# Kernel optimization log

Measured on AMD Instinct MI355X. Metric: run time of the kernel, lower is better.

The kernel has to match this reference:

```python
import jax, jax.numpy as jnp
import numpy as np

NB, H = 4, 16
EPS = 1e-5


def _ln(x, w=None, b=None):
    m = jnp.mean(x, -1, keepdims=True)
    v = jnp.var(x, -1, keepdims=True)
    y = (x - m) * jax.lax.rsqrt(v + EPS)
    if w is not None:
        y = y * w
    if b is not None:
        y = y + b
    return y


def _ada_ln(a, s, ln_s_w, w_gamma, w_beta):
    # AF3 Algorithm 26: a <- sigmoid(Lin(LN_nobias(s))) * LN_noaffine(a) + Lin(LN_nobias(s))
    a_n = _ln(a)
    s_n = _ln(s, ln_s_w)
    return jax.nn.sigmoid(s_n @ w_gamma) * a_n + s_n @ w_beta


def setup_inputs():
    key = jax.random.key(0)
    B, S, c_a, c_s, c_z = 1, 1024, 768, 384, 128
    n_hidden = 2 * c_a  # expansion factor n=2
    ks = iter(jax.random.split(key, 40))

    def rn(shape, scale=1.0):
        return scale * jax.random.normal(next(ks), shape, dtype=jnp.float32)

    p = 0.02
    return {
        "a": rn((B, S, c_a)),
        "s": rn((B, S, c_s)),
        "z": rn((B, S, S, c_z)),
        "beta": rn((B, S, S, H)),
        # per-block AttentionPairBias params (stacked over NB blocks)
        "ln_s_w_attn": jnp.ones((NB, c_s)),
        "wg_attn": rn((NB, c_s, c_a), p),
        "wb_attn": rn((NB, c_s, c_a), p),
        "wq": rn((NB, c_a, c_a), p),
        "bq": jnp.zeros((NB, c_a)),
        "wk": rn((NB, c_a, c_a), p),
        "wv": rn((NB, c_a, c_a), p),
        "ln_z_w": jnp.ones((NB, c_z)),
        "ln_z_b": jnp.zeros((NB, c_z)),
        "wpb": rn((NB, c_z, H), p),
        "wgate": rn((NB, c_a, c_a), p),
        "wo": rn((NB, c_a, c_a), p),
        "wsg_attn": rn((NB, c_s, c_a), p),
        "bsg_attn": -2.0 * jnp.ones((NB, c_a)),
        # per-block ConditionedTransitionBlock params
        "ln_s_w_tr": jnp.ones((NB, c_s)),
        "wg_tr": rn((NB, c_s, c_a), p),
        "wb_tr": rn((NB, c_s, c_a), p),
        "w_swish": rn((NB, c_a, n_hidden), p),
        "w_gate2": rn((NB, c_a, n_hidden), p),
        "wsg_tr": rn((NB, c_s, c_a), p),
        "bsg_tr": -2.0 * jnp.ones((NB, c_a)),
        "w_out": rn((NB, n_hidden, c_a), p),
    }


def reference(a, s, z, beta, ln_s_w_attn, wg_attn, wb_attn, wq, bq, wk, wv,
              ln_z_w, ln_z_b, wpb, wgate, wo, wsg_attn, bsg_attn,
              ln_s_w_tr, wg_tr, wb_tr, w_swish, w_gate2, wsg_tr, bsg_tr, w_out):
    B, S, c_a = a.shape
    d = c_a // H
    scale = 1.0 / jnp.sqrt(jnp.float32(d))
    for i in range(NB):
        # --- AttentionPairBias (AF3 Alg 24) ---
        ah = _ada_ln(a, s, ln_s_w_attn[i], wg_attn[i], wb_attn[i])
        q = (ah @ wq[i] + bq[i]).reshape(B, S, H, d)
        k = (ah @ wk[i]).reshape(B, S, H, d)
        v = (ah @ wv[i]).reshape(B, S, H, d)
        zb = _ln(z, ln_z_w[i], ln_z_b[i]) @ wpb[i]  # [B,S,S,H] pair bias
        scores = jnp.einsum('bihd,bjhd->bhij', q, k) * scale \
                 + jnp.transpose(zb + beta, (0, 3, 1, 2))
        attn = jax.nn.softmax(scores, axis=-1)
        o = jnp.einsum('bhij,bjhd->bihd', attn, v)
        g = jax.nn.sigmoid(ah @ wgate[i]).reshape(B, S, H, d)
        att_out = (g * o).reshape(B, S, c_a) @ wo[i]
        b_attn = jax.nn.sigmoid(s @ wsg_attn[i] + bsg_attn[i]) * att_out
        # --- ConditionedTransitionBlock (AF3 Alg 25, SwiGLU) ---
        th = _ada_ln(a, s, ln_s_w_tr[i], wg_tr[i], wb_tr[i])
        hidden = jax.nn.silu(th @ w_swish[i]) * (th @ w_gate2[i])
        tr = jax.nn.sigmoid(s @ wsg_tr[i] + bsg_tr[i]) * (hidden @ w_out[i])
        a = b_attn + tr
    return a
```

## Files before the change

### kernel.cpp

```cpp
#include <hip/hip_runtime.h>
#include <hip/hip_bf16.h>

typedef __hip_bfloat16 bf16;
typedef __attribute__((ext_vector_type(8))) short s8v;
typedef __attribute__((ext_vector_type(4))) float f4v;

constexpr int S = 1024, CA = 768, CS = 384, CZ = 128, NHID = 1536;
constexpr int NBLK = 4, NHEAD = 16, DH = 48;
constexpr float EPS = 1e-5f;

#define DEV static __device__ __forceinline__

DEV float sigmoidf_(float x) { return 1.0f / (1.0f + __expf(-x)); }

DEV f4v mfma16(s8v a, s8v b, f4v c) {
  return __builtin_amdgcn_mfma_f32_16x16x32_bf16(a, b, c, 0, 0, 0);
}

DEV void gld_lds16(const void* g, void* l) {
  __builtin_amdgcn_global_load_lds((const __attribute__((address_space(1))) void*)g,
                                   (__attribute__((address_space(3))) void*)l, 16, 0, 0);
}

union U8 { s8v s; bf16 h[8]; };
union U4 { uint2 u; bf16 h[4]; };

DEV float wred_sum(float v) {
#pragma unroll
  for (int o = 32; o; o >>= 1) v += __shfl_xor(v, o);
  return v;
}

__global__ __launch_bounds__(256) void rowln_s(const float* __restrict__ x,
                                               bf16* __restrict__ s_hat,
                                               bf16* __restrict__ s_bf) {
  constexpr int C = CS, C4 = C / 4;
  __shared__ float red[8];
  const int t = threadIdx.x;
  const size_t row = blockIdx.x;
  float4 v = make_float4(0.f, 0.f, 0.f, 0.f);
  if (t < C4) v = ((const float4*)(x + row * C))[t];
  float sum = v.x + v.y + v.z + v.w;
  float sq = v.x * v.x + v.y * v.y + v.z * v.z + v.w * v.w;
  sum = wred_sum(sum); sq = wred_sum(sq);
  const int wv = t >> 6;
  if ((t & 63) == 0) { red[2 * wv] = sum; red[2 * wv + 1] = sq; }
  __syncthreads();
  sum = red[0] + red[2] + red[4] + red[6];
  sq = red[1] + red[3] + red[5] + red[7];
  const float m = sum / C;
  const float rstd = rsqrtf(sq / C - m * m + EPS);
  if (t < C4) {
    U4 oh, ob_;
    oh.h[0] = __float2bfloat16((v.x - m) * rstd); oh.h[1] = __float2bfloat16((v.y - m) * rstd);
    oh.h[2] = __float2bfloat16((v.z - m) * rstd); oh.h[3] = __float2bfloat16((v.w - m) * rstd);
    ob_.h[0] = __float2bfloat16(v.x); ob_.h[1] = __float2bfloat16(v.y);
    ob_.h[2] = __float2bfloat16(v.z); ob_.h[3] = __float2bfloat16(v.w);
    *(uint2*)(s_hat + row * C + 4 * t) = oh.u;
    *(uint2*)(s_bf + row * C + 4 * t) = ob_.u;
  }
}

__global__ __launch_bounds__(256) void ln_adaln2(const float* __restrict__ a,
                                                 const bf16* __restrict__ ada,
                                                 bf16* __restrict__ ah_attn,
                                                 bf16* __restrict__ ah_tr) {
  __shared__ float red[8];
  const int t = threadIdx.x;
  const size_t row = blockIdx.x;
  float4 v = make_float4(0.f, 0.f, 0.f, 0.f);
  if (t < 192) v = ((const float4*)(a + row * CA))[t];
  float sum = v.x + v.y + v.z + v.w;
  float sq = v.x * v.x + v.y * v.y + v.z * v.z + v.w * v.w;
  sum = wred_sum(sum); sq = wred_sum(sq);
  const int wv = t >> 6;
  if ((t & 63) == 0) { red[2 * wv] = sum; red[2 * wv + 1] = sq; }
  __syncthreads();
  sum = red[0] + red[2] + red[4] + red[6];
  sq = red[1] + red[3] + red[5] + red[7];
  const float m = sum / CA;
  const float rstd = rsqrtf(sq / CA - m * m + EPS);
  if (t < 192) {
    const float an[4] = {(v.x - m) * rstd, (v.y - m) * rstd, (v.z - m) * rstd, (v.w - m) * rstd};
    const bf16* ar = ada + row * 12288 + 4 * t;
    U4 g1, b1, g2, b2, o1, o2;
    g1.u = *(const uint2*)(ar);
    b1.u = *(const uint2*)(ar + 768);
    g2.u = *(const uint2*)(ar + 1536);
    b2.u = *(const uint2*)(ar + 2304);
#pragma unroll
    for (int j = 0; j < 4; ++j) {
      o1.h[j] = __float2bfloat16(sigmoidf_(__bfloat162float(g1.h[j])) * an[j] + __bfloat162float(b1.h[j]));
      o2.h[j] = __float2bfloat16(sigmoidf_(__bfloat162float(g2.h[j])) * an[j] + __bfloat162float(b2.h[j]));
    }
    *(uint2*)(ah_attn + row * CA + 4 * t) = o1.u;
    *(uint2*)(ah_tr + row * CA + 4 * t) = o2.u;
  }
}

__global__ __launch_bounds__(256) void final_adaln(const float* __restrict__ sg,
                                                   const bf16* __restrict__ att,
                                                   const bf16* __restrict__ tr,
                                                   const bf16* __restrict__ ada,
                                                   bf16* __restrict__ ah_attn,
                                                   bf16* __restrict__ ah_tr) {
  __shared__ float red[8];
  const int t = threadIdx.x;
  const size_t row = blockIdx.x;
  float o[4] = {0.f, 0.f, 0.f, 0.f};
  if (t < 192) {
    const float4 sa = *(const float4*)(sg + row * 6144 + 4 * t);
    const float4 st = *(const float4*)(sg + row * 6144 + 768 + 4 * t);
    U4 av, tv;
    av.u = *(const uint2*)(att + row * CA + 4 * t);
    tv.u = *(const uint2*)(tr + row * CA + 4 * t);
    o[0] = sa.x * __bfloat162float(av.h[0]) + st.x * __bfloat162float(tv.h[0]);
    o[1] = sa.y * __bfloat162float(av.h[1]) + st.y * __bfloat162float(tv.h[1]);
    o[2] = sa.z * __bfloat162float(av.h[2]) + st.z * __bfloat162float(tv.h[2]);
    o[3] = sa.w * __bfloat162float(av.h[3]) + st.w * __bfloat162float(tv.h[3]);
  }
  float sum = o[0] + o[1] + o[2] + o[3];
  float sq = o[0] * o[0] + o[1] * o[1] + o[2] * o[2] + o[3] * o[3];
  sum = wred_sum(sum); sq = wred_sum(sq);
  const int wv = t >> 6;
  if ((t & 63) == 0) { red[2 * wv] = sum; red[2 * wv + 1] = sq; }
  __syncthreads();
  sum = red[0] + red[2] + red[4] + red[6];
  sq = red[1] + red[3] + red[5] + red[7];
  const float m = sum / CA;
  const float rstd = rsqrtf(sq / CA - m * m + EPS);
  if (t < 192) {
    const bf16* ar = ada + row * 12288 + 4 * t;
    U4 g1, b1, g2, b2, o1, o2;
    g1.u = *(const uint2*)(ar);
    b1.u = *(const uint2*)(ar + 768);
    g2.u = *(const uint2*)(ar + 1536);
    b2.u = *(const uint2*)(ar + 2304);
#pragma unroll
    for (int j = 0; j < 4; ++j) {
      const float an = (o[j] - m) * rstd;
      o1.h[j] = __float2bfloat16(sigmoidf_(__bfloat162float(g1.h[j])) * an + __bfloat162float(b1.h[j]));
      o2.h[j] = __float2bfloat16(sigmoidf_(__bfloat162float(g2.h[j])) * an + __bfloat162float(b2.h[j]));
    }
    *(uint2*)(ah_attn + row * CA + 4 * t) = o1.u;
    *(uint2*)(ah_tr + row * CA + 4 * t) = o2.u;
  }
}

struct TGroup {
  const float* src[6];
  bf16* dst[6];
  const float* cs[6];
  long dstZ[6];
};

__global__ __launch_bounds__(256) void transpose_grp(TGroup g, int K, int N, int csZ) {
  __shared__ float tile[32][33];
  const int z = blockIdx.z, wsel = z >> 2, blk = z & 3;
  const float* src = g.src[wsel] + (size_t)blk * K * N;
  bf16* dst = g.dst[wsel] + (size_t)blk * g.dstZ[wsel];
  const float* cs = g.cs[wsel];
  const int k0 = blockIdx.y * 32, n0 = blockIdx.x * 32;
  const int tx = threadIdx.x & 31, ty = threadIdx.x >> 5;
#pragma unroll
  for (int q = 0; q < 4; ++q) {
    const int k = k0 + ty + 8 * q;
    float v = src[(size_t)k * N + n0 + tx];
    if (cs) v *= cs[(size_t)blk * csZ + k];
    tile[ty + 8 * q][tx] = v;
  }
  __syncthreads();
#pragma unroll
  for (int q = 0; q < 4; ++q)
    dst[(size_t)(n0 + ty + 8 * q) * K + k0 + tx] = __float2bfloat16(tile[tx][ty + 8 * q]);
}

__global__ __launch_bounds__(256) void prep_all(const float* __restrict__ ln_z_w,
                                                const float* __restrict__ ln_z_b,
                                                const float* __restrict__ wpb,
                                                bf16* __restrict__ W2T,
                                                float* __restrict__ bias2,
                                                const float* __restrict__ bq,
                                                const float* __restrict__ bsg_attn,
                                                const float* __restrict__ bsg_tr,
                                                float* __restrict__ biasQKVG,
                                                float* __restrict__ biasSG) {
  const int blk = blockIdx.x;
  const int t = threadIdx.x;
  if (blk == 48) {
    for (int f = t; f < 64 * CZ; f += 256) {
      const int col = f >> 7, c = f & 127, b = col >> 4, h = col & 15;
      W2T[f] = __float2bfloat16(ln_z_w[b * CZ + c] * wpb[(b * CZ + c) * NHEAD + h]);
    }
    if (t < 64) {
      const int b = t >> 4, h = t & 15;
      float sum = 0.f;
      for (int c = 0; c < CZ; ++c)
        sum += ln_z_b[b * CZ + c] * wpb[(b * CZ + c) * NHEAD + h];
      bias2[t] = sum;
    }
    return;
  }
  const int g = blk * 256 + t;
  if (g < 4 * 3072) {
    const int b = g / 3072, c = g % 3072;
    biasQKVG[g] = (c < 768) ? bq[b * 768 + c] : 0.f;
  }
  if (g < 6144) {
    const int b = g / 1536, c = g % 1536;
    biasSG[g] = (c < 768) ? bsg_attn[b * 768 + c] : bsg_tr[b * 768 + c - 768];
  }
}

__global__ __launch_bounds__(256) void zbias_kernel(const float* __restrict__ z,
                                                    const float* __restrict__ beta,
                                                    const bf16* __restrict__ W2T,
                                                    const float* __restrict__ bias2,
                                                    bf16* __restrict__ bias_all) {
  __shared__ s8v zt8[64 * 16];
  __shared__ s8v w2s[64 * 16];
  __shared__ float betas[64][17];
  __shared__ float bias2s[64];
  __shared__ bf16 obuf[64][72];
  const int t = threadIdx.x;
  const int i = blockIdx.y, j0 = blockIdx.x * 64;
#pragma unroll
  for (int q = 0; q < 4; ++q) {
    const int u = q * 256 + t;
    const int row = u >> 4, sl = u & 15;
    w2s[row * 16 + (sl ^ (row & 7))] = *(const s8v*)(W2T + row * CZ + sl * 8);
  }
  if (t < 64) bias2s[t] = bias2[t];
  {
    const int j = t >> 2, h4 = t & 3;
    const float4 bv = *(const float4*)(beta + ((size_t)i * S + j0 + j) * NHEAD + 4 * h4);
    betas[j][4 * h4 + 0] = bv.x; betas[j][4 * h4 + 1] = bv.y;
    betas[j][4 * h4 + 2] = bv.z; betas[j][4 * h4 + 3] = bv.w;
  }
  {
    const int p = t >> 2, q = t & 3;
    const float* zr = z + ((size_t)i * S + j0 + p) * CZ + q * 32;
    float vals[32];
    float sum = 0.f, sq = 0.f;
#pragma unroll
    for (int k4 = 0; k4 < 8; ++k4) {
      const float4 xv = *(const float4*)(zr + 4 * k4);
      vals[4 * k4 + 0] = xv.x; vals[4 * k4 + 1] = xv.y;
      vals[4 * k4 + 2] = xv.z; vals[4 * k4 + 3] = xv.w;
      sum += xv.x + xv.y + xv.z + xv.w;
      sq += xv.x * xv.x + xv.y * xv.y + xv.z * xv.z + xv.w * xv.w;
    }
    sum += __shfl_xor(sum, 1); sum += __shfl_xor(sum, 2);
    sq += __shfl_xor(sq, 1); sq += __shfl_xor(sq, 2);
    const float m = sum / CZ;
    const float rstd = rsqrtf(sq / CZ - m * m + EPS);
#pragma unroll
    for (int u = 0; u < 4; ++u) {
      U8 pk;
#pragma unroll
      for (int e = 0; e < 8; ++e) pk.h[e] = __float2bfloat16((vals[8 * u + e] - m) * rstd);
      const int cu = 4 * q + u;
      zt8[p * 16 + (cu ^ (p & 7))] = pk.s;
    }
  }
  __syncthreads();
  const int lane = t & 63, wid = t >> 6;
  const int wr = wid >> 1, wc = wid & 1;
  const int ln = lane & 15, lq = lane >> 4;
  f4v acc[2][2] = {};
#pragma unroll
  for (int kk = 0; kk < 4; ++kk) {
    const int sl = (lq + 4 * kk) ^ (ln & 7);
    s8v a[2], b[2];
#pragma unroll
    for (int mi = 0; mi < 2; ++mi) a[mi] = zt8[(32 * wr + 16 * mi + ln) * 16 + sl];
#pragma unroll
    for (int ni = 0; ni < 2; ++ni) b[ni] = w2s[(32 * wc + 16 * ni + ln) * 16 + sl];
#pragma unroll
    for (int mi = 0; mi < 2; ++mi)
#pragma unroll
      for (int ni = 0; ni < 2; ++ni) acc[mi][ni] = mfma16(a[mi], b[ni], acc[mi][ni]);
  }
#pragma unroll
  for (int mi = 0; mi < 2; ++mi)
#pragma unroll
    for (int ni = 0; ni < 2; ++ni) {
      const int col = 32 * wc + 16 * ni + ln;
      const int jb = 32 * wr + 16 * mi + 4 * lq;
      U4 o4;
#pragma unroll
      for (int r = 0; r < 4; ++r)
        o4.h[r] = __float2bfloat16(acc[mi][ni][r] + bias2s[col] + betas[jb + r][col & 15]);
      *(uint2*)&obuf[col][jb] = o4.u;
    }
  __syncthreads();
  {
    const int oc = t >> 2, js = (t & 3) * 16;
    bf16* dp = bias_all + (size_t)oc * S * S + (size_t)i * S + j0 + js;
    *(s8v*)dp = *(const s8v*)&obuf[oc][js];
    *(s8v*)(dp + 8) = *(const s8v*)&obuf[oc][js + 8];
  }
}

struct Gemm2Args {
  const bf16* A0[2]; int lda0[2];
  const bf16* Bt[2];
  const float* bias[2];
  void* C[2];
  int K[2];
  int nb[2];
  int outMode[2];
  int N[2];
  bf16* vT;
};

__global__ __launch_bounds__(256) void gemm2(Gemm2Args ga) {
  const int z = blockIdx.z;
  if ((int)blockIdx.x >= ga.nb[z]) return;
  __shared__ s8v As[1024];
  __shared__ s8v Bs[1024];
  const bf16* A0 = ga.A0[z]; const int lda0 = ga.lda0[z];
  const bf16* Bt = ga.Bt[z];
  const int K = ga.K[z], N = ga.N[z];
  const int t = threadIdx.x;
  const int lane = t & 63, wid = t >> 6;
  const int wr = wid >> 1, wc = wid & 1;
  const int ln = lane & 15, lq = lane >> 4;
  const int m0 = blockIdx.y * 128, n0 = blockIdx.x * 128;
  int rowA[4], colx[4];
#pragma unroll
  for (int q = 0; q < 4; ++q) {
    const int u = q * 256 + t, row = u >> 3, slp = u & 7;
    rowA[q] = row; colx[q] = (slp ^ (row & 7)) * 8;
  }
  f4v acc[4][4] = {};
  for (int ks = 0; ks < K; ks += 64) {
    __syncthreads();
#pragma unroll
    for (int q = 0; q < 4; ++q) {
      gld_lds16(A0 + (size_t)(m0 + rowA[q]) * lda0 + ks + colx[q], &As[q * 256 + wid * 64]);
      gld_lds16(Bt + (size_t)(n0 + rowA[q]) * K + ks + colx[q], &Bs[q * 256 + wid * 64]);
    }
    __syncthreads();
#pragma unroll
    for (int kk = 0; kk < 2; ++kk) {
      const int sl = (lq + 4 * kk) ^ (ln & 7);
      s8v a[4], b[4];
#pragma unroll
      for (int mi = 0; mi < 4; ++mi) a[mi] = As[(64 * wr + 16 * mi + ln) * 8 + sl];
#pragma unroll
      for (int ni = 0; ni < 4; ++ni) b[ni] = Bs[(64 * wc + 16 * ni + ln) * 8 + sl];
#pragma unroll
      for (int mi = 0; mi < 4; ++mi)
#pragma unroll
        for (int ni = 0; ni < 4; ++ni) acc[mi][ni] = mfma16(a[mi], b[ni], acc[mi][ni]);
    }
  }
  const bool vdiv = (ga.vT != nullptr) && (z == 0) && (n0 >= 1536) && (n0 < 2304);
  const int om = ga.outMode[z];
#pragma unroll
  for (int ni = 0; ni < 4; ++ni) {
    const int n = n0 + 64 * wc + 16 * ni + ln;
    const float bv = ga.bias[z] ? ga.bias[z][n] : 0.f;
#pragma unroll
    for (int mi = 0; mi < 4; ++mi) {
      const int mb = m0 + 64 * wr + 16 * mi + 4 * lq;
      if (vdiv) {
        U4 o4;
#pragma unroll
        for (int r = 0; r < 4; ++r) o4.h[r] = __float2bfloat16(acc[mi][ni][r] + bv);
        *(uint2*)(ga.vT + (size_t)(n - 1536) * S + mb) = o4.u;
      } else if (om == 0) {
        bf16* C = (bf16*)ga.C[z];
#pragma unroll
        for (int r = 0; r < 4; ++r)
          C[(size_t)(mb + r) * N + n] = __float2bfloat16(acc[mi][ni][r] + bv);
      } else {
        float* C = (float*)ga.C[z];
#pragma unroll
        for (int r = 0; r < 4; ++r)
          C[(size_t)(mb + r) * N + n] = sigmoidf_(acc[mi][ni][r] + bv);
      }
    }
  }
}

struct GemmPairArgs {
  const bf16* A0[2]; int lda0[2];
  const bf16* A1[2]; int lda1[2];
  const bf16* Bt[2];
  const float* bias[2];
  bf16* C[2];
  int K[2]; int amode[2];
};

DEV s8v combineRT(s8v x, s8v y, int amode) {
  U8 ux, uy, r;
  ux.s = x; uy.s = y;
#pragma unroll
  for (int j = 0; j < 8; ++j) {
    const float fx = __bfloat162float(ux.h[j]);
    const float fy = __bfloat162float(uy.h[j]);
    const float tt = sigmoidf_(fx);
    r.h[j] = __float2bfloat16((amode == 2 ? fx * tt : tt) * fy);
  }
  return r.s;
}

__global__ __launch_bounds__(256) void gemm_pair(GemmPairArgs ga, int N) {
  __shared__ s8v As[128 * 8];
  __shared__ s8v Bs[128 * 8];
  const int z = blockIdx.z;
  const bf16* A0 = ga.A0[z]; const int lda0 = ga.lda0[z];
  const bf16* A1 = ga.A1[z]; const int lda1 = ga.lda1[z];
  const bf16* Bt = ga.Bt[z];
  const float* bias = ga.bias[z];
  bf16* C = ga.C[z];
  const int K = ga.K[z], amode = ga.amode[z];
  const int t = threadIdx.x;
  const int lane = t & 63, wid = t >> 6;
  const int wr = wid >> 1, wc = wid & 1;
  const int ln = lane & 15, lq = lane >> 4;
  const int m0 = blockIdx.y * 128, n0 = blockIdx.x * 128;
  int rowS[4], slS[4], swz[4];
#pragma unroll
  for (int q = 0; q < 4; ++q) {
    const int u = q * 256 + t;
    rowS[q] = u >> 3; slS[q] = u & 7;
    swz[q] = rowS[q] * 8 + (slS[q] ^ (rowS[q] & 7));
  }
  f4v acc[4][4] = {};
  s8v ra[4], ra2[4], rb[4];
#pragma unroll
  for (int q = 0; q < 4; ++q) {
    ra[q] = *(const s8v*)(A0 + (size_t)(m0 + rowS[q]) * lda0 + slS[q] * 8);
    if (amode != 0) ra2[q] = *(const s8v*)(A1 + (size_t)(m0 + rowS[q]) * lda1 + slS[q] * 8);
    rb[q] = *(const s8v*)(Bt + (size_t)(n0 + rowS[q]) * K + slS[q] * 8);
  }
  for (int ks = 0;;) {
    __syncthreads();
#pragma unroll
    for (int q = 0; q < 4; ++q) {
      As[swz[q]] = (amode == 0) ? ra[q] : combineRT(ra[q], ra2[q], amode);
      Bs[swz[q]] = rb[q];
    }
    const int ksn = ks + 64;
    if (ksn < K) {
#pragma unroll
      for (int q = 0; q < 4; ++q) {
        ra[q] = *(const s8v*)(A0 + (size_t)(m0 + rowS[q]) * lda0 + ksn + slS[q] * 8);
        if (amode != 0) ra2[q] = *(const s8v*)(A1 + (size_t)(m0 + rowS[q]) * lda1 + ksn + slS[q] * 8);
        rb[q] = *(const s8v*)(Bt + (size_t)(n0 + rowS[q]) * K + ksn + slS[q] * 8);
      }
    }
    __syncthreads();
#pragma unroll
    for (int kk = 0; kk < 2; ++kk) {
      const int sl = (lq + 4 * kk) ^ (ln & 7);
      s8v a[4], b[4];
#pragma unroll
      for (int mi = 0; mi < 4; ++mi) a[mi] = As[(64 * wr + 16 * mi + ln) * 8 + sl];
#pragma unroll
      for (int ni = 0; ni < 4; ++ni) b[ni] = Bs[(64 * wc + 16 * ni + ln) * 8 + sl];
#pragma unroll
      for (int mi = 0; mi < 4; ++mi)
#pragma unroll
        for (int ni = 0; ni < 4; ++ni) acc[mi][ni] = mfma16(a[mi], b[ni], acc[mi][ni]);
    }
    ks = ksn;
    if (ks >= K) break;
  }
#pragma unroll
  for (int ni = 0; ni < 4; ++ni) {
    const int n = n0 + 64 * wc + 16 * ni + ln;
    const float bv = bias ? bias[n] : 0.f;
#pragma unroll
    for (int mi = 0; mi < 4; ++mi) {
      const int mb = m0 + 64 * wr + 16 * mi + 4 * lq;
#pragma unroll
      for (int r = 0; r < 4; ++r)
        C[(size_t)(mb + r) * N + n] = __float2bfloat16(acc[mi][ni][r] + bv);
    }
  }
}

__global__ __launch_bounds__(256) void flash_attn(const bf16* __restrict__ qkvg,
                                                  const bf16* __restrict__ vT,
                                                  const bf16* __restrict__ bias_all,
                                                  bf16* __restrict__ ob, int blk) {
  __shared__ s8v Qs[64 * 8];
  __shared__ s8v Ks[2][64 * 8];
  __shared__ s8v Vs[2][48 * 8];
  __shared__ s8v Bs[2][64 * 8];
  __shared__ bf16 PwB[4 * 1024];
  __shared__ float facL[4][16];
  __shared__ float linvL[4][16];
  const int t = threadIdx.x;
  const int lane = t & 63, w = t >> 6;
  const int ln = lane & 15, lq = lane >> 4;
  const int h = blockIdx.y, i0 = blockIdx.x * 64;
  const bf16* bp = bias_all + (size_t)(blk * NHEAD + h) * S * S;
  const float scale = 0.14433756729740643f;

#pragma unroll
  for (int uu = 0; uu < 2; ++uu) {
    const int u = t + 256 * uu, row = u >> 3, sl = u & 7;
    s8v qv{};
    if (sl < 6) qv = *(const s8v*)(qkvg + (size_t)(i0 + row) * 3072 + h * DH + sl * 8);
    Qs[row * 8 + (sl ^ (row & 7))] = qv;
  }

  s8v kr[2], br[2], vr0{}, vr1{};
  auto prefetch = [&](int jt) {
    const int j0 = jt * 64;
#pragma unroll
    for (int uu = 0; uu < 2; ++uu) {
      const int u = t + 256 * uu, row = u >> 3, sl = u & 7;
      s8v kv{};
      if (sl < 6) kv = *(const s8v*)(qkvg + (size_t)(j0 + row) * 3072 + 768 + h * DH + sl * 8);
      kr[uu] = kv;
      br[uu] = *(const s8v*)(bp + (size_t)(i0 + row) * S + j0 + sl * 8);
    }
    { const int d = t >> 3, sl = t & 7;
      vr0 = *(const s8v*)(vT + (size_t)(h * DH + d) * S + j0 + sl * 8); }
    if (t < 128) {
      const int u = 256 + t, d = u >> 3, sl = u & 7;
      vr1 = *(const s8v*)(vT + (size_t)(h * DH + d) * S + j0 + sl * 8);
    }
  };
  auto store_tiles = [&](int pb) {
#pragma unroll
    for (int uu = 0; uu < 2; ++uu) {
      const int u = t + 256 * uu, row = u >> 3, sl = u & 7;
      const int ph = row * 8 + (sl ^ (row & 7));
      Ks[pb][ph] = kr[uu];
      Bs[pb][ph] = br[uu];
    }
    { const int d = t >> 3, sl = t & 7;
      Vs[pb][d * 8 + (sl ^ (d & 7))] = vr0; }
    if (t < 128) {
      const int u = 256 + t, d = u >> 3, sl = u & 7;
      Vs[pb][d * 8 + (sl ^ (d & 7))] = vr1;
    }
  };

  float m_run = -3e30f, l_run = 0.f;
  f4v acc_o[3] = {};
  bf16* pw = PwB + w * 1024;

  prefetch(0);
  for (int jt = 0; jt < 16; ++jt) {
    const int pb = jt & 1;
    __syncthreads();
    store_tiles(pb);
    __syncthreads();
    if (jt < 15) prefetch(jt + 1);
    float p[4][4];
    float tmax = -3e30f;
#pragma unroll
    for (int ja = 0; ja < 4; ++ja) {
      f4v accs = {};
#pragma unroll
      for (int ks2 = 0; ks2 < 2; ++ks2) {
        const int sl = (lq + 4 * ks2) ^ (ln & 7);
        const s8v a = Ks[pb][(16 * ja + ln) * 8 + sl];
        const s8v b = Qs[(16 * w + ln) * 8 + sl];
        accs = mfma16(a, b, accs);
      }
      const int jq = 4 * ja + lq;
      const int pu = jq >> 1;
      U4 bv;
      bv.u = *(const uint2*)((const bf16*)(&Bs[pb][0]) +
                             (((16 * w + ln) * 8 + (pu ^ (ln & 7))) * 8 + (jq & 1) * 4));
#pragma unroll
      for (int r = 0; r < 4; ++r) {
        p[ja][r] = accs[r] * scale + __bfloat162float(bv.h[r]);
        tmax = fmaxf(tmax, p[ja][r]);
      }
    }
    tmax = fmaxf(tmax, __shfl_xor(tmax, 16));
    tmax = fmaxf(tmax, __shfl_xor(tmax, 32));
    const float m_new = fmaxf(m_run, tmax);
    const float fac = __expf(m_run - m_new);
    m_run = m_new;
    float psum = 0.f;
#pragma unroll
    for (int ja = 0; ja < 4; ++ja)
#pragma unroll
      for (int r = 0; r < 4; ++r) {
        p[ja][r] = __expf(p[ja][r] - m_new);
        psum += p[ja][r];
      }
    psum += __shfl_xor(psum, 16);
    psum += __shfl_xor(psum, 32);
    l_run = l_run * fac + psum;
    if (lq == 0) facL[w][ln] = fac;
#pragma unroll
    for (int ja = 0; ja < 4; ++ja) {
      const int ju = 4 * ja + lq;
      const int ph = ju ^ ((ln & 7) << 1);
      U4 pk;
#pragma unroll
      for (int r = 0; r < 4; ++r) pk.h[r] = __float2bfloat16(p[ja][r]);
      *(uint2*)(pw + ln * 64 + ph * 4) = pk.u;
    }
    asm volatile("s_waitcnt lgkmcnt(0)" ::: "memory");
    __builtin_amdgcn_sched_barrier(0);
    const float4 fv = *(const float4*)&facL[w][4 * lq];
#pragma unroll
    for (int ni = 0; ni < 3; ++ni) {
      acc_o[ni][0] *= fv.x; acc_o[ni][1] *= fv.y;
      acc_o[ni][2] *= fv.z; acc_o[ni][3] *= fv.w;
    }
#pragma unroll
    for (int ks2 = 0; ks2 < 2; ++ks2) {
      const int pu0 = (2 * lq + 8 * ks2) ^ ((ln & 7) << 1);
      const s8v pa = *(const s8v*)(pw + ln * 64 + pu0 * 4);
      const int slv = (lq + 4 * ks2) ^ (ln & 7);
#pragma unroll
      for (int ni = 0; ni < 3; ++ni) {
        const s8v vb = Vs[pb][(16 * ni + ln) * 8 + slv];
        acc_o[ni] = mfma16(pa, vb, acc_o[ni]);
      }
    }
  }
  if (lq == 0) linvL[w][ln] = 1.0f / l_run;
  asm volatile("s_waitcnt lgkmcnt(0)" ::: "memory");
  __builtin_amdgcn_sched_barrier(0);
  const float4 lv = *(const float4*)&linvL[w][4 * lq];
  const float lvr[4] = {lv.x, lv.y, lv.z, lv.w};
#pragma unroll
  for (int ni = 0; ni < 3; ++ni)
#pragma unroll
    for (int r = 0; r < 4; ++r) {
      const int m = i0 + 16 * w + 4 * lq + r;
      ob[(size_t)m * CA + h * DH + 16 * ni + ln] = __float2bfloat16(acc_o[ni][r] * lvr[r]);
    }
}

__global__ __launch_bounds__(256) void ew_final(const float* __restrict__ sg,
                                                const bf16* __restrict__ att,
                                                const bf16* __restrict__ tr,
                                                float* __restrict__ out) {
  const int i = blockIdx.x * 256 + threadIdx.x;
  const int row = i / 192, col = (i % 192) * 4;
  const float4 sa = *(const float4*)(sg + (size_t)row * 6144 + col);
  const float4 st = *(const float4*)(sg + (size_t)row * 6144 + 768 + col);
  U4 av, tv;
  av.u = *(const uint2*)(att + (size_t)row * CA + col);
  tv.u = *(const uint2*)(tr + (size_t)row * CA + col);
  float4 o;
  o.x = sa.x * __bfloat162float(av.h[0]) + st.x * __bfloat162float(tv.h[0]);
  o.y = sa.y * __bfloat162float(av.h[1]) + st.y * __bfloat162float(tv.h[1]);
  o.z = sa.z * __bfloat162float(av.h[2]) + st.z * __bfloat162float(tv.h[2]);
  o.w = sa.w * __bfloat162float(av.h[3]) + st.w * __bfloat162float(tv.h[3]);
  *(float4*)(out + (size_t)row * CA + col) = o;
}

__global__ void fill_kernel(float* p, int n, float v) {
  const int i = blockIdx.x * 256 + threadIdx.x;
  if (i < n) p[i] = v;
}

extern "C" void kernel_launch(void* const* d_in, const int* in_sizes, int n_in,
                              void* d_out, int out_size, void* d_ws, size_t ws_size,
                              hipStream_t stream) {
  (void)in_sizes; (void)n_in;
  const float* a_in = (const float*)d_in[0];
  const float* s_in = (const float*)d_in[1];
  const float* z_in = (const float*)d_in[2];
  const float* beta = (const float*)d_in[3];
  const float* ln_s_w_attn = (const float*)d_in[4];
  const float* wg_attn = (const float*)d_in[5];
  const float* wb_attn = (const float*)d_in[6];
  const float* wq = (const float*)d_in[7];
  const float* bq = (const float*)d_in[8];
  const float* wk = (const float*)d_in[9];
  const float* wv = (const float*)d_in[10];
  const float* ln_z_w = (const float*)d_in[11];
  const float* ln_z_b = (const float*)d_in[12];
  const float* wpb = (const float*)d_in[13];
  const float* wgate = (const float*)d_in[14];
  const float* wo = (const float*)d_in[15];
  const float* wsg_attn = (const float*)d_in[16];
  const float* bsg_attn = (const float*)d_in[17];
  const float* ln_s_w_tr = (const float*)d_in[18];
  const float* wg_tr = (const float*)d_in[19];
  const float* wb_tr = (const float*)d_in[20];
  const float* w_swish = (const float*)d_in[21];
  const float* w_gate2 = (const float*)d_in[22];
  const float* wsg_tr = (const float*)d_in[23];
  const float* bsg_tr = (const float*)d_in[24];
  const float* w_out = (const float*)d_in[25];

  char* wp = (char*)d_ws;
  size_t used = 0;
  auto alloc = [&](size_t bytes) -> void* {
    void* p = wp + used;
    used += (bytes + 255) & ~(size_t)255;
    return p;
  };
  bf16* bias_all = (bf16*)alloc((size_t)64 * S * S * 2);
  bf16* WT_ada = (bf16*)alloc((size_t)4 * 3072 * 384 * 2);
  bf16* WT_sg = (bf16*)alloc((size_t)4 * 1536 * 384 * 2);
  bf16* WT_qkvg = (bf16*)alloc((size_t)4 * 3072 * 768 * 2);
  bf16* WT_wo = (bf16*)alloc((size_t)4 * 768 * 768 * 2);
  bf16* WT_mlp = (bf16*)alloc((size_t)4 * 3072 * 768 * 2);
  bf16* WT_wout = (bf16*)alloc((size_t)4 * 768 * 1536 * 2);
  float* biasQKVG = (float*)alloc(4 * 3072 * 4);
  float* biasSG = (float*)alloc(6144 * 4);
  bf16* W2T = (bf16*)alloc(64 * 128 * 2);
  float* bias2 = (float*)alloc(64 * 4);
  bf16* ada_all = (bf16*)alloc((size_t)S * 12288 * 2);
  float* sg_all = (float*)alloc((size_t)S * 6144 * 4);
  bf16* s_hat = (bf16*)alloc((size_t)S * CS * 2);
  bf16* s_bf = (bf16*)alloc((size_t)S * CS * 2);
  bf16* ah_attn = (bf16*)alloc((size_t)S * CA * 2);
  bf16* ah_tr = (bf16*)alloc((size_t)S * CA * 2);
  bf16* qkvg = (bf16*)alloc((size_t)S * 3072 * 2);
  bf16* vT = (bf16*)alloc((size_t)CA * S * 2);
  bf16* ob = (bf16*)alloc((size_t)S * CA * 2);
  bf16* att = (bf16*)alloc((size_t)S * CA * 2);
  bf16* swg = (bf16*)alloc((size_t)S * 3072 * 2);
  bf16* trout = (bf16*)alloc((size_t)S * CA * 2);
  if (used > ws_size) {
    fill_kernel<<<(out_size + 255) / 256, 256, 0, stream>>>((float*)d_out, out_size, 12345.0f);
    return;
  }

  const dim3 B256(256);

  prep_all<<<49, B256, 0, stream>>>(ln_z_w, ln_z_b, wpb, W2T, bias2,
                                    bq, bsg_attn, bsg_tr, biasQKVG, biasSG);

  {
    TGroup g{};
    g.src[0] = wg_attn;  g.dst[0] = WT_ada + (size_t)0 * 384;    g.cs[0] = ln_s_w_attn; g.dstZ[0] = 3072 * 384;
    g.src[1] = wb_attn;  g.dst[1] = WT_ada + (size_t)768 * 384;  g.cs[1] = ln_s_w_attn; g.dstZ[1] = 3072 * 384;
    g.src[2] = wg_tr;    g.dst[2] = WT_ada + (size_t)1536 * 384; g.cs[2] = ln_s_w_tr;   g.dstZ[2] = 3072 * 384;
    g.src[3] = wb_tr;    g.dst[3] = WT_ada + (size_t)2304 * 384; g.cs[3] = ln_s_w_tr;   g.dstZ[3] = 3072 * 384;
    g.src[4] = wsg_attn; g.dst[4] = WT_sg + (size_t)0 * 384;     g.cs[4] = nullptr;     g.dstZ[4] = 1536 * 384;
    g.src[5] = wsg_tr;   g.dst[5] = WT_sg + (size_t)768 * 384;   g.cs[5] = nullptr;     g.dstZ[5] = 1536 * 384;
    transpose_grp<<<dim3(24, 12, 24), B256, 0, stream>>>(g, 384, 768, CS);
  }
  {
    TGroup g{};
    g.src[0] = wq;    g.dst[0] = WT_qkvg + (size_t)0 * 768;    g.dstZ[0] = 3072 * 768;
    g.src[1] = wk;    g.dst[1] = WT_qkvg + (size_t)768 * 768;  g.dstZ[1] = 3072 * 768;
    g.src[2] = wv;    g.dst[2] = WT_qkvg + (size_t)1536 * 768; g.dstZ[2] = 3072 * 768;
    g.src[3] = wgate; g.dst[3] = WT_qkvg + (size_t)2304 * 768; g.dstZ[3] = 3072 * 768;
    g.src[4] = wo;    g.dst[4] = WT_wo;                        g.dstZ[4] = 768 * 768;
    transpose_grp<<<dim3(24, 24, 20), B256, 0, stream>>>(g, 768, 768, 0);
  }
  {
    TGroup g{};
    g.src[0] = w_swish; g.dst[0] = WT_mlp + (size_t)0 * 768;    g.dstZ[0] = 3072 * 768;
    g.src[1] = w_gate2; g.dst[1] = WT_mlp + (size_t)1536 * 768; g.dstZ[1] = 3072 * 768;
    transpose_grp<<<dim3(48, 24, 8), B256, 0, stream>>>(g, 768, 1536, 0);
  }
  {
    TGroup g{};
    g.src[0] = w_out; g.dst[0] = WT_wout; g.dstZ[0] = 768 * 1536;
    transpose_grp<<<dim3(24, 48, 4), B256, 0, stream>>>(g, 1536, 768, 0);
  }

  rowln_s<<<S, B256, 0, stream>>>(s_in, s_hat, s_bf);
  zbias_kernel<<<dim3(16, 1024), B256, 0, stream>>>(z_in, beta, W2T, bias2, bias_all);

  {
    Gemm2Args ga{};
    ga.A0[0] = s_hat; ga.lda0[0] = 384; ga.Bt[0] = WT_ada; ga.bias[0] = nullptr;
    ga.C[0] = ada_all; ga.K[0] = 384; ga.nb[0] = 96; ga.outMode[0] = 0; ga.N[0] = 12288;
    ga.A0[1] = s_bf; ga.lda0[1] = 384; ga.Bt[1] = WT_sg; ga.bias[1] = biasSG;
    ga.C[1] = sg_all; ga.K[1] = 384; ga.nb[1] = 48; ga.outMode[1] = 1; ga.N[1] = 6144;
    ga.vT = nullptr;
    gemm2<<<dim3(96, 8, 2), B256, 0, stream>>>(ga);
  }

  ln_adaln2<<<S, B256, 0, stream>>>(a_in, ada_all, ah_attn, ah_tr);
  for (int b = 0; b < NBLK; ++b) {
    {
      Gemm2Args ga{};
      ga.A0[0] = ah_attn; ga.lda0[0] = 768; ga.Bt[0] = WT_qkvg + (size_t)b * 3072 * 768;
      ga.bias[0] = biasQKVG + b * 3072; ga.C[0] = qkvg; ga.K[0] = 768; ga.nb[0] = 24;
      ga.outMode[0] = 0; ga.N[0] = 3072;
      ga.A0[1] = ah_tr; ga.lda0[1] = 768; ga.Bt[1] = WT_mlp + (size_t)b * 3072 * 768;
      ga.bias[1] = nullptr; ga.C[1] = swg; ga.K[1] = 768; ga.nb[1] = 24;
      ga.outMode[1] = 0; ga.N[1] = 3072;
      ga.vT = vT;
      gemm2<<<dim3(24, 8, 2), B256, 0, stream>>>(ga);
    }
    flash_attn<<<dim3(16, 16), B256, 0, stream>>>(qkvg, vT, bias_all, ob, b);
    {
      GemmPairArgs ga{};
      ga.A0[0] = qkvg + 2304; ga.lda0[0] = 3072; ga.A1[0] = ob; ga.lda1[0] = 768;
      ga.Bt[0] = WT_wo + (size_t)b * 768 * 768; ga.bias[0] = nullptr;
      ga.C[0] = att; ga.K[0] = 768; ga.amode[0] = 1;
      ga.A0[1] = swg; ga.lda0[1] = 3072; ga.A1[1] = swg + 1536; ga.lda1[1] = 3072;
      ga.Bt[1] = WT_wout + (size_t)b * 768 * 1536; ga.bias[1] = nullptr;
      ga.C[1] = trout; ga.K[1] = 1536; ga.amode[1] = 2;
      gemm_pair<<<dim3(6, 8, 2), B256, 0, stream>>>(ga, 768);
    }
    if (b < NBLK - 1) {
      final_adaln<<<S, B256, 0, stream>>>(sg_all + (size_t)b * 1536, att, trout,
                                          ada_all + (size_t)(b + 1) * 3072, ah_attn, ah_tr);
    } else {
      ew_final<<<768, B256, 0, stream>>>(sg_all + (size_t)b * 1536, att, trout, (float*)d_out);
    }
  }
}
```

Measured before the change: 676.6 us.

## Split flash attention over key halves and unify GEMMs with smaller M tiles

Flash attention now runs as two key-range halves per query tile, writing partial fp32 outputs and (max, sum) stats that a new combine kernel merges into the normalized bf16 output. This doubles the number of attention workgroups from 256 to 512 to better fill the GPU. All GEMMs go through a single gemmA kernel whose grid uses 16 row blocks instead of 8, so each tile covers 64 rows and more blocks run at once. The cost is an extra kernel launch, fp32 partial output traffic, and possibly less data reuse per GEMM tile.

```diff
diff --git a/kernel.cpp b/kernel.cpp
--- a/kernel.cpp
+++ b/kernel.cpp
@@ -15,11 +15,6 @@
 
 DEV f4v mfma16(s8v a, s8v b, f4v c) {
   return __builtin_amdgcn_mfma_f32_16x16x32_bf16(a, b, c, 0, 0, 0);
-}
-
-DEV void gld_lds16(const void* g, void* l) {
-  __builtin_amdgcn_global_load_lds((const __attribute__((address_space(1))) void*)g,
-                                   (__attribute__((address_space(3))) void*)l, 16, 0, 0);
 }
 
 union U8 { s8v s; bf16 h[8]; };
@@ -147,497 +142,6 @@
   }
 }
 
-struct TGroup {
-  const float* src[6];
-  bf16* dst[6];
-  const float* cs[6];
-  long dstZ[6];
-};
-
-__global__ __launch_bounds__(256) void transpose_grp(TGroup g, int K, int N, int csZ) {
-  __shared__ float tile[32][33];
-  const int z = blockIdx.z, wsel = z >> 2, blk = z & 3;
-  const float* src = g.src[wsel] + (size_t)blk * K * N;
-  bf16* dst = g.dst[wsel] + (size_t)blk * g.dstZ[wsel];
-  const float* cs = g.cs[wsel];
-  const int k0 = blockIdx.y * 32, n0 = blockIdx.x * 32;
-  const int tx = threadIdx.x & 31, ty = threadIdx.x >> 5;
-#pragma unroll
-  for (int q = 0; q < 4; ++q) {
-    const int k = k0 + ty + 8 * q;
-    float v = src[(size_t)k * N + n0 + tx];
-    if (cs) v *= cs[(size_t)blk * csZ + k];
-    tile[ty + 8 * q][tx] = v;
-  }
-  __syncthreads();
-#pragma unroll
-  for (int q = 0; q < 4; ++q)
-    dst[(size_t)(n0 + ty + 8 * q) * K + k0 + tx] = __float2bfloat16(tile[tx][ty + 8 * q]);
-}
-
-__global__ __launch_bounds__(256) void prep_all(const float* __restrict__ ln_z_w,
-                                                const float* __restrict__ ln_z_b,
-                                                const float* __restrict__ wpb,
-                                                bf16* __restrict__ W2T,
-                                                float* __restrict__ bias2,
-                                                const float* __restrict__ bq,
-                                                const float* __restrict__ bsg_attn,
-                                                const float* __restrict__ bsg_tr,
-                                                float* __restrict__ biasQKVG,
-                                                float* __restrict__ biasSG) {
-  const int blk = blockIdx.x;
-  const int t = threadIdx.x;
-  if (blk == 48) {
-    for (int f = t; f < 64 * CZ; f += 256) {
-      const int col = f >> 7, c = f & 127, b = col >> 4, h = col & 15;
-      W2T[f] = __float2bfloat16(ln_z_w[b * CZ + c] * wpb[(b * CZ + c) * NHEAD + h]);
-    }
-    if (t < 64) {
-      const int b = t >> 4, h = t & 15;
-      float sum = 0.f;
-      for (int c = 0; c < CZ; ++c)
-        sum += ln_z_b[b * CZ + c] * wpb[(b * CZ + c) * NHEAD + h];
-      bias2[t] = sum;
-    }
-    return;
-  }
-  const int g = blk * 256 + t;
-  if (g < 4 * 3072) {
-    const int b = g / 3072, c = g % 3072;
-    biasQKVG[g] = (c < 768) ? bq[b * 768 + c] : 0.f;
-  }
-  if (g < 6144) {
-    const int b = g / 1536, c = g % 1536;
-    biasSG[g] = (c < 768) ? bsg_attn[b * 768 + c] : bsg_tr[b * 768 + c - 768];
-  }
-}
-
-__global__ __launch_bounds__(256) void zbias_kernel(const float* __restrict__ z,
-                                                    const float* __restrict__ beta,
-                                                    const bf16* __restrict__ W2T,
-                                                    const float* __restrict__ bias2,
-                                                    bf16* __restrict__ bias_all) {
-  __shared__ s8v zt8[64 * 16];
-  __shared__ s8v w2s[64 * 16];
-  __shared__ float betas[64][17];
-  __shared__ float bias2s[64];
-  __shared__ bf16 obuf[64][72];
-  const int t = threadIdx.x;
-  const int i = blockIdx.y, j0 = blockIdx.x * 64;
-#pragma unroll
-  for (int q = 0; q < 4; ++q) {
-    const int u = q * 256 + t;
-    const int row = u >> 4, sl = u & 15;
-    w2s[row * 16 + (sl ^ (row & 7))] = *(const s8v*)(W2T + row * CZ + sl * 8);
-  }
-  if (t < 64) bias2s[t] = bias2[t];
-  {
-    const int j = t >> 2, h4 = t & 3;
-    const float4 bv = *(const float4*)(beta + ((size_t)i * S + j0 + j) * NHEAD + 4 * h4);
-    betas[j][4 * h4 + 0] = bv.x; betas[j][4 * h4 + 1] = bv.y;
-    betas[j][4 * h4 + 2] = bv.z; betas[j][4 * h4 + 3] = bv.w;
-  }
-  {
-    const int p = t >> 2, q = t & 3;
-    const float* zr = z + ((size_t)i * S + j0 + p) * CZ + q * 32;
-    float vals[32];
-    float sum = 0.f, sq = 0.f;
-#pragma unroll
-    for (int k4 = 0; k4 < 8; ++k4) {
-      const float4 xv = *(const float4*)(zr + 4 * k4);
-      vals[4 * k4 + 0] = xv.x; vals[4 * k4 + 1] = xv.y;
-      vals[4 * k4 + 2] = xv.z; vals[4 * k4 + 3] = xv.w;
-      sum += xv.x + xv.y + xv.z + xv.w;
-      sq += xv.x * xv.x + xv.y * xv.y + xv.z * xv.z + xv.w * xv.w;
-    }
-    sum += __shfl_xor(sum, 1); sum += __shfl_xor(sum, 2);
-    sq += __shfl_xor(sq, 1); sq += __shfl_xor(sq, 2);
-    const float m = sum / CZ;
-    const float rstd = rsqrtf(sq / CZ - m * m + EPS);
-#pragma unroll
-    for (int u = 0; u < 4; ++u) {
-      U8 pk;
-#pragma unroll
-      for (int e = 0; e < 8; ++e) pk.h[e] = __float2bfloat16((vals[8 * u + e] - m) * rstd);
-      const int cu = 4 * q + u;
-      zt8[p * 16 + (cu ^ (p & 7))] = pk.s;
-    }
-  }
-  __syncthreads();
-  const int lane = t & 63, wid = t >> 6;
-  const int wr = wid >> 1, wc = wid & 1;
-  const int ln = lane & 15, lq = lane >> 4;
-  f4v acc[2][2] = {};
-#pragma unroll
-  for (int kk = 0; kk < 4; ++kk) {
-    const int sl = (lq + 4 * kk) ^ (ln & 7);
-    s8v a[2], b[2];
-#pragma unroll
-    for (int mi = 0; mi < 2; ++mi) a[mi] = zt8[(32 * wr + 16 * mi + ln) * 16 + sl];
-#pragma unroll
-    for (int ni = 0; ni < 2; ++ni) b[ni] = w2s[(32 * wc + 16 * ni + ln) * 16 + sl];
-#pragma unroll
-    for (int mi = 0; mi < 2; ++mi)
-#pragma unroll
-      for (int ni = 0; ni < 2; ++ni) acc[mi][ni] = mfma16(a[mi], b[ni], acc[mi][ni]);
-  }
-#pragma unroll
-  for (int mi = 0; mi < 2; ++mi)
-#pragma unroll
-    for (int ni = 0; ni < 2; ++ni) {
-      const int col = 32 * wc + 16 * ni + ln;
-      const int jb = 32 * wr + 16 * mi + 4 * lq;
-      U4 o4;
-#pragma unroll
-      for (int r = 0; r < 4; ++r)
-        o4.h[r] = __float2bfloat16(acc[mi][ni][r] + bias2s[col] + betas[jb + r][col & 15]);
-      *(uint2*)&obuf[col][jb] = o4.u;
-    }
-  __syncthreads();
-  {
-    const int oc = t >> 2, js = (t & 3) * 16;
-    bf16* dp = bias_all + (size_t)oc * S * S + (size_t)i * S + j0 + js;
-    *(s8v*)dp = *(const s8v*)&obuf[oc][js];
-    *(s8v*)(dp + 8) = *(const s8v*)&obuf[oc][js + 8];
-  }
-}
-
-struct Gemm2Args {
-  const bf16* A0[2]; int lda0[2];
-  const bf16* Bt[2];
-  const float* bias[2];
-  void* C[2];
-  int K[2];
-  int nb[2];
-  int outMode[2];
-  int N[2];
-  bf16* vT;
-};
-
-__global__ __launch_bounds__(256) void gemm2(Gemm2Args ga) {
-  const int z = blockIdx.z;
-  if ((int)blockIdx.x >= ga.nb[z]) return;
-  __shared__ s8v As[1024];
-  __shared__ s8v Bs[1024];
-  const bf16* A0 = ga.A0[z]; const int lda0 = ga.lda0[z];
-  const bf16* Bt = ga.Bt[z];
-  const int K = ga.K[z], N = ga.N[z];
-  const int t = threadIdx.x;
-  const int lane = t & 63, wid = t >> 6;
-  const int wr = wid >> 1, wc = wid & 1;
-  const int ln = lane & 15, lq = lane >> 4;
-  const int m0 = blockIdx.y * 128, n0 = blockIdx.x * 128;
-  int rowA[4], colx[4];
-#pragma unroll
-  for (int q = 0; q < 4; ++q) {
-    const int u = q * 256 + t, row = u >> 3, slp = u & 7;
-    rowA[q] = row; colx[q] = (slp ^ (row & 7)) * 8;
-  }
-  f4v acc[4][4] = {};
-  for (int ks = 0; ks < K; ks += 64) {
-    __syncthreads();
-#pragma unroll
-    for (int q = 0; q < 4; ++q) {
-      gld_lds16(A0 + (size_t)(m0 + rowA[q]) * lda0 + ks + colx[q], &As[q * 256 + wid * 64]);
-      gld_lds16(Bt + (size_t)(n0 + rowA[q]) * K + ks + colx[q], &Bs[q * 256 + wid * 64]);
-    }
-    __syncthreads();
-#pragma unroll
-    for (int kk = 0; kk < 2; ++kk) {
-      const int sl = (lq + 4 * kk) ^ (ln & 7);
-      s8v a[4], b[4];
-#pragma unroll
-      for (int mi = 0; mi < 4; ++mi) a[mi] = As[(64 * wr + 16 * mi + ln) * 8 + sl];
-#pragma unroll
-      for (int ni = 0; ni < 4; ++ni) b[ni] = Bs[(64 * wc + 16 * ni + ln) * 8 + sl];
-#pragma unroll
-      for (int mi = 0; mi < 4; ++mi)
-#pragma unroll
-        for (int ni = 0; ni < 4; ++ni) acc[mi][ni] = mfma16(a[mi], b[ni], acc[mi][ni]);
-    }
-  }
-  const bool vdiv = (ga.vT != nullptr) && (z == 0) && (n0 >= 1536) && (n0 < 2304);
-  const int om = ga.outMode[z];
-#pragma unroll
-  for (int ni = 0; ni < 4; ++ni) {
-    const int n = n0 + 64 * wc + 16 * ni + ln;
-    const float bv = ga.bias[z] ? ga.bias[z][n] : 0.f;
-#pragma unroll
-    for (int mi = 0; mi < 4; ++mi) {
-      const int mb = m0 + 64 * wr + 16 * mi + 4 * lq;
-      if (vdiv) {
-        U4 o4;
-#pragma unroll
-        for (int r = 0; r < 4; ++r) o4.h[r] = __float2bfloat16(acc[mi][ni][r] + bv);
-        *(uint2*)(ga.vT + (size_t)(n - 1536) * S + mb) = o4.u;
-      } else if (om == 0) {
-        bf16* C = (bf16*)ga.C[z];
-#pragma unroll
-        for (int r = 0; r < 4; ++r)
-          C[(size_t)(mb + r) * N + n] = __float2bfloat16(acc[mi][ni][r] + bv);
-      } else {
-        float* C = (float*)ga.C[z];
-#pragma unroll
-        for (int r = 0; r < 4; ++r)
-          C[(size_t)(mb + r) * N + n] = sigmoidf_(acc[mi][ni][r] + bv);
-      }
-    }
-  }
-}
-
-struct GemmPairArgs {
-  const bf16* A0[2]; int lda0[2];
-  const bf16* A1[2]; int lda1[2];
-  const bf16* Bt[2];
-  const float* bias[2];
-  bf16* C[2];
-  int K[2]; int amode[2];
-};
-
-DEV s8v combineRT(s8v x, s8v y, int amode) {
-  U8 ux, uy, r;
-  ux.s = x; uy.s = y;
-#pragma unroll
-  for (int j = 0; j < 8; ++j) {
-    const float fx = __bfloat162float(ux.h[j]);
-    const float fy = __bfloat162float(uy.h[j]);
-    const float tt = sigmoidf_(fx);
-    r.h[j] = __float2bfloat16((amode == 2 ? fx * tt : tt) * fy);
-  }
-  return r.s;
-}
-
-__global__ __launch_bounds__(256) void gemm_pair(GemmPairArgs ga, int N) {
-  __shared__ s8v As[128 * 8];
-  __shared__ s8v Bs[128 * 8];
-  const int z = blockIdx.z;
-  const bf16* A0 = ga.A0[z]; const int lda0 = ga.lda0[z];
-  const bf16* A1 = ga.A1[z]; const int lda1 = ga.lda1[z];
-  const bf16* Bt = ga.Bt[z];
-  const float* bias = ga.bias[z];
-  bf16* C = ga.C[z];
-  const int K = ga.K[z], amode = ga.amode[z];
-  const int t = threadIdx.x;
-  const int lane = t & 63, wid = t >> 6;
-  const int wr = wid >> 1, wc = wid & 1;
-  const int ln = lane & 15, lq = lane >> 4;
-  const int m0 = blockIdx.y * 128, n0 = blockIdx.x * 128;
-  int rowS[4], slS[4], swz[4];
-#pragma unroll
-  for (int q = 0; q < 4; ++q) {
-    const int u = q * 256 + t;
-    rowS[q] = u >> 3; slS[q] = u & 7;
-    swz[q] = rowS[q] * 8 + (slS[q] ^ (rowS[q] & 7));
-  }
-  f4v acc[4][4] = {};
-  s8v ra[4], ra2[4], rb[4];
-#pragma unroll
-  for (int q = 0; q < 4; ++q) {
-    ra[q] = *(const s8v*)(A0 + (size_t)(m0 + rowS[q]) * lda0 + slS[q] * 8);
-    if (amode != 0) ra2[q] = *(const s8v*)(A1 + (size_t)(m0 + rowS[q]) * lda1 + slS[q] * 8);
-    rb[q] = *(const s8v*)(Bt + (size_t)(n0 + rowS[q]) * K + slS[q] * 8);
-  }
-  for (int ks = 0;;) {
-    __syncthreads();
-#pragma unroll
-    for (int q = 0; q < 4; ++q) {
-      As[swz[q]] = (amode == 0) ? ra[q] : combineRT(ra[q], ra2[q], amode);
-      Bs[swz[q]] = rb[q];
-    }
-    const int ksn = ks + 64;
-    if (ksn < K) {
-#pragma unroll
-      for (int q = 0; q < 4; ++q) {
-        ra[q] = *(const s8v*)(A0 + (size_t)(m0 + rowS[q]) * lda0 + ksn + slS[q] * 8);
-        if (amode != 0) ra2[q] = *(const s8v*)(A1 + (size_t)(m0 + rowS[q]) * lda1 + ksn + slS[q] * 8);
-        rb[q] = *(const s8v*)(Bt + (size_t)(n0 + rowS[q]) * K + ksn + slS[q] * 8);
-      }
-    }
-    __syncthreads();
-#pragma unroll
-    for (int kk = 0; kk < 2; ++kk) {
-      const int sl = (lq + 4 * kk) ^ (ln & 7);
-      s8v a[4], b[4];
-#pragma unroll
-      for (int mi = 0; mi < 4; ++mi) a[mi] = As[(64 * wr + 16 * mi + ln) * 8 + sl];
-#pragma unroll
-      for (int ni = 0; ni < 4; ++ni) b[ni] = Bs[(64 * wc + 16 * ni + ln) * 8 + sl];
-#pragma unroll
-      for (int mi = 0; mi < 4; ++mi)
-#pragma unroll
-        for (int ni = 0; ni < 4; ++ni) acc[mi][ni] = mfma16(a[mi], b[ni], acc[mi][ni]);
-    }
-    ks = ksn;
-    if (ks >= K) break;
-  }
-#pragma unroll
-  for (int ni = 0; ni < 4; ++ni) {
-    const int n = n0 + 64 * wc + 16 * ni + ln;
-    const float bv = bias ? bias[n] : 0.f;
-#pragma unroll
-    for (int mi = 0; mi < 4; ++mi) {
-      const int mb = m0 + 64 * wr + 16 * mi + 4 * lq;
-#pragma unroll
-      for (int r = 0; r < 4; ++r)
-        C[(size_t)(mb + r) * N + n] = __float2bfloat16(acc[mi][ni][r] + bv);
-    }
-  }
-}
-
-__global__ __launch_bounds__(256) void flash_attn(const bf16* __restrict__ qkvg,
-                                                  const bf16* __restrict__ vT,
-                                                  const bf16* __restrict__ bias_all,
-                                                  bf16* __restrict__ ob, int blk) {
-  __shared__ s8v Qs[64 * 8];
-  __shared__ s8v Ks[2][64 * 8];
-  __shared__ s8v Vs[2][48 * 8];
-  __shared__ s8v Bs[2][64 * 8];
-  __shared__ bf16 PwB[4 * 1024];
-  __shared__ float facL[4][16];
-  __shared__ float linvL[4][16];
-  const int t = threadIdx.x;
-  const int lane = t & 63, w = t >> 6;
-  const int ln = lane & 15, lq = lane >> 4;
-  const int h = blockIdx.y, i0 = blockIdx.x * 64;
-  const bf16* bp = bias_all + (size_t)(blk * NHEAD + h) * S * S;
-  const float scale = 0.14433756729740643f;
-
-#pragma unroll
-  for (int uu = 0; uu < 2; ++uu) {
-    const int u = t + 256 * uu, row = u >> 3, sl = u & 7;
-    s8v qv{};
-    if (sl < 6) qv = *(const s8v*)(qkvg + (size_t)(i0 + row) * 3072 + h * DH + sl * 8);
-    Qs[row * 8 + (sl ^ (row & 7))] = qv;
-  }
-
-  s8v kr[2], br[2], vr0{}, vr1{};
-  auto prefetch = [&](int jt) {
-    const int j0 = jt * 64;
-#pragma unroll
-    for (int uu = 0; uu < 2; ++uu) {
-      const int u = t + 256 * uu, row = u >> 3, sl = u & 7;
-      s8v kv{};
-      if (sl < 6) kv = *(const s8v*)(qkvg + (size_t)(j0 + row) * 3072 + 768 + h * DH + sl * 8);
-      kr[uu] = kv;
-      br[uu] = *(const s8v*)(bp + (size_t)(i0 + row) * S + j0 + sl * 8);
-    }
-    { const int d = t >> 3, sl = t & 7;
-      vr0 = *(const s8v*)(vT + (size_t)(h * DH + d) * S + j0 + sl * 8); }
-    if (t < 128) {
-      const int u = 256 + t, d = u >> 3, sl = u & 7;
-      vr1 = *(const s8v*)(vT + (size_t)(h * DH + d) * S + j0 + sl * 8);
-    }
-  };
-  auto store_tiles = [&](int pb) {
-#pragma unroll
-    for (int uu = 0; uu < 2; ++uu) {
-      const int u = t + 256 * uu, row = u >> 3, sl = u & 7;
-      const int ph = row * 8 + (sl ^ (row & 7));
-      Ks[pb][ph] = kr[uu];
-      Bs[pb][ph] = br[uu];
-    }
-    { const int d = t >> 3, sl = t & 7;
-      Vs[pb][d * 8 + (sl ^ (d & 7))] = vr0; }
-    if (t < 128) {
-      const int u = 256 + t, d = u >> 3, sl = u & 7;
-      Vs[pb][d * 8 + (sl ^ (d & 7))] = vr1;
-    }
-  };
-
-  float m_run = -3e30f, l_run = 0.f;
-  f4v acc_o[3] = {};
-  bf16* pw = PwB + w * 1024;
-
-  prefetch(0);
-  for (int jt = 0; jt < 16; ++jt) {
-    const int pb = jt & 1;
-    __syncthreads();
-    store_tiles(pb);
-    __syncthreads();
-    if (jt < 15) prefetch(jt + 1);
-    float p[4][4];
-    float tmax = -3e30f;
-#pragma unroll
-    for (int ja = 0; ja < 4; ++ja) {
-      f4v accs = {};
-#pragma unroll
-      for (int ks2 = 0; ks2 < 2; ++ks2) {
-        const int sl = (lq + 4 * ks2) ^ (ln & 7);
-        const s8v a = Ks[pb][(16 * ja + ln) * 8 + sl];
-        const s8v b = Qs[(16 * w + ln) * 8 + sl];
-        accs = mfma16(a, b, accs);
-      }
-      const int jq = 4 * ja + lq;
-      const int pu = jq >> 1;
-      U4 bv;
-      bv.u = *(const uint2*)((const bf16*)(&Bs[pb][0]) +
-                             (((16 * w + ln) * 8 + (pu ^ (ln & 7))) * 8 + (jq & 1) * 4));
-#pragma unroll
-      for (int r = 0; r < 4; ++r) {
-        p[ja][r] = accs[r] * scale + __bfloat162float(bv.h[r]);
-        tmax = fmaxf(tmax, p[ja][r]);
-      }
-    }
-    tmax = fmaxf(tmax, __shfl_xor(tmax, 16));
-    tmax = fmaxf(tmax, __shfl_xor(tmax, 32));
-    const float m_new = fmaxf(m_run, tmax);
-    const float fac = __expf(m_run - m_new);
-    m_run = m_new;
-    float psum = 0.f;
-#pragma unroll
-    for (int ja = 0; ja < 4; ++ja)
-#pragma unroll
-      for (int r = 0; r < 4; ++r) {
-        p[ja][r] = __expf(p[ja][r] - m_new);
-        psum += p[ja][r];
-      }
-    psum += __shfl_xor(psum, 16);
-    psum += __shfl_xor(psum, 32);
-    l_run = l_run * fac + psum;
-    if (lq == 0) facL[w][ln] = fac;
-#pragma unroll
-    for (int ja = 0; ja < 4; ++ja) {
-      const int ju = 4 * ja + lq;
-      const int ph = ju ^ ((ln & 7) << 1);
-      U4 pk;
-#pragma unroll
-      for (int r = 0; r < 4; ++r) pk.h[r] = __float2bfloat16(p[ja][r]);
-      *(uint2*)(pw + ln * 64 + ph * 4) = pk.u;
-    }
-    asm volatile("s_waitcnt lgkmcnt(0)" ::: "memory");
-    __builtin_amdgcn_sched_barrier(0);
-    const float4 fv = *(const float4*)&facL[w][4 * lq];
-#pragma unroll
-    for (int ni = 0; ni < 3; ++ni) {
-      acc_o[ni][0] *= fv.x; acc_o[ni][1] *= fv.y;
-      acc_o[ni][2] *= fv.z; acc_o[ni][3] *= fv.w;
-    }
-#pragma unroll
-    for (int ks2 = 0; ks2 < 2; ++ks2) {
-      const int pu0 = (2 * lq + 8 * ks2) ^ ((ln & 7) << 1);
-      const s8v pa = *(const s8v*)(pw + ln * 64 + pu0 * 4);
-      const int slv = (lq + 4 * ks2) ^ (ln & 7);
-#pragma unroll
-      for (int ni = 0; ni < 3; ++ni) {
-        const s8v vb = Vs[pb][(16 * ni + ln) * 8 + slv];
-        acc_o[ni] = mfma16(pa, vb, acc_o[ni]);
-      }
-    }
-  }
-  if (lq == 0) linvL[w][ln] = 1.0f / l_run;
-  asm volatile("s_waitcnt lgkmcnt(0)" ::: "memory");
-  __builtin_amdgcn_sched_barrier(0);
-  const float4 lv = *(const float4*)&linvL[w][4 * lq];
-  const float lvr[4] = {lv.x, lv.y, lv.z, lv.w};
-#pragma unroll
-  for (int ni = 0; ni < 3; ++ni)
-#pragma unroll
-    for (int r = 0; r < 4; ++r) {
-      const int m = i0 + 16 * w + 4 * lq + r;
-      ob[(size_t)m * CA + h * DH + 16 * ni + ln] = __float2bfloat16(acc_o[ni][r] * lvr[r]);
-    }
-}
-
 __global__ __launch_bounds__(256) void ew_final(const float* __restrict__ sg,
                                                 const bf16* __restrict__ att,
                                                 const bf16* __restrict__ tr,
@@ -655,6 +159,462 @@
   o.z = sa.z * __bfloat162float(av.h[2]) + st.z * __bfloat162float(tv.h[2]);
   o.w = sa.w * __bfloat162float(av.h[3]) + st.w * __bfloat162float(tv.h[3]);
   *(float4*)(out + (size_t)row * CA + col) = o;
+}
+
+struct TGroup {
+  const float* src[6];
+  bf16* dst[6];
+  const float* cs[6];
+  long dstZ[6];
+};
+
+__global__ __launch_bounds__(256) void transpose_grp(TGroup g, int K, int N, int csZ) {
+  __shared__ float tile[32][33];
+  const int z = blockIdx.z, wsel = z >> 2, blk = z & 3;
+  const float* src = g.src[wsel] + (size_t)blk * K * N;
+  bf16* dst = g.dst[wsel] + (size_t)blk * g.dstZ[wsel];
+  const float* cs = g.cs[wsel];
+  const int k0 = blockIdx.y * 32, n0 = blockIdx.x * 32;
+  const int tx = threadIdx.x & 31, ty = threadIdx.x >> 5;
+#pragma unroll
+  for (int q = 0; q < 4; ++q) {
+    const int k = k0 + ty + 8 * q;
+    float v = src[(size_t)k * N + n0 + tx];
+    if (cs) v *= cs[(size_t)blk * csZ + k];
+    tile[ty + 8 * q][tx] = v;
+  }
+  __syncthreads();
+#pragma unroll
+  for (int q = 0; q < 4; ++q)
+    dst[(size_t)(n0 + ty + 8 * q) * K + k0 + tx] = __float2bfloat16(tile[tx][ty + 8 * q]);
+}
+
+__global__ __launch_bounds__(256) void prep_all(const float* __restrict__ ln_z_w,
+                                                const float* __restrict__ ln_z_b,
+                                                const float* __restrict__ wpb,
+                                                bf16* __restrict__ W2T,
+                                                float* __restrict__ bias2,
+                                                const float* __restrict__ bq,
+                                                const float* __restrict__ bsg_attn,
+                                                const float* __restrict__ bsg_tr,
+                                                float* __restrict__ biasQKVG,
+                                                float* __restrict__ biasSG) {
+  const int blk = blockIdx.x;
+  const int t = threadIdx.x;
+  if (blk == 48) {
+    for (int f = t; f < 64 * CZ; f += 256) {
+      const int col = f >> 7, c = f & 127, b = col >> 4, h = col & 15;
+      W2T[f] = __float2bfloat16(ln_z_w[b * CZ + c] * wpb[(b * CZ + c) * NHEAD + h]);
+    }
+    if (t < 64) {
+      const int b = t >> 4, h = t & 15;
+      float sum = 0.f;
+      for (int c = 0; c < CZ; ++c)
+        sum += ln_z_b[b * CZ + c] * wpb[(b * CZ + c) * NHEAD + h];
+      bias2[t] = sum;
+    }
+    return;
+  }
+  const int g = blk * 256 + t;
+  if (g < 4 * 3072) {
+    const int b = g / 3072, c = g % 3072;
+    biasQKVG[g] = (c < 768) ? bq[b * 768 + c] : 0.f;
+  }
+  if (g < 6144) {
+    const int b = g / 1536, c = g % 1536;
+    biasSG[g] = (c < 768) ? bsg_attn[b * 768 + c] : bsg_tr[b * 768 + c - 768];
+  }
+}
+
+__global__ __launch_bounds__(256) void zbias_kernel(const float* __restrict__ z,
+                                                    const float* __restrict__ beta,
+                                                    const bf16* __restrict__ W2T,
+                                                    const float* __restrict__ bias2,
+                                                    bf16* __restrict__ bias_all) {
+  __shared__ s8v zt8[64 * 16];
+  __shared__ s8v w2s[64 * 16];
+  __shared__ float betas[64][17];
+  __shared__ float bias2s[64];
+  __shared__ bf16 obuf[64][72];
+  const int t = threadIdx.x;
+  const int i = blockIdx.y, j0 = blockIdx.x * 64;
+#pragma unroll
+  for (int q = 0; q < 4; ++q) {
+    const int u = q * 256 + t;
+    const int row = u >> 4, sl = u & 15;
+    w2s[row * 16 + (sl ^ (row & 7))] = *(const s8v*)(W2T + row * CZ + sl * 8);
+  }
+  if (t < 64) bias2s[t] = bias2[t];
+  {
+    const int j = t >> 2, h4 = t & 3;
+    const float4 bv = *(const float4*)(beta + ((size_t)i * S + j0 + j) * NHEAD + 4 * h4);
+    betas[j][4 * h4 + 0] = bv.x; betas[j][4 * h4 + 1] = bv.y;
+    betas[j][4 * h4 + 2] = bv.z; betas[j][4 * h4 + 3] = bv.w;
+  }
+  {
+    const int p = t >> 2, q = t & 3;
+    const float* zr = z + ((size_t)i * S + j0 + p) * CZ + q * 32;
+    float vals[32];
+    float sum = 0.f, sq = 0.f;
+#pragma unroll
+    for (int k4 = 0; k4 < 8; ++k4) {
+      const float4 xv = *(const float4*)(zr + 4 * k4);
+      vals[4 * k4 + 0] = xv.x; vals[4 * k4 + 1] = xv.y;
+      vals[4 * k4 + 2] = xv.z; vals[4 * k4 + 3] = xv.w;
+      sum += xv.x + xv.y + xv.z + xv.w;
+      sq += xv.x * xv.x + xv.y * xv.y + xv.z * xv.z + xv.w * xv.w;
+    }
+    sum += __shfl_xor(sum, 1); sum += __shfl_xor(sum, 2);
+    sq += __shfl_xor(sq, 1); sq += __shfl_xor(sq, 2);
+    const float m = sum / CZ;
+    const float rstd = rsqrtf(sq / CZ - m * m + EPS);
+#pragma unroll
+    for (int u = 0; u < 4; ++u) {
+      U8 pk;
+#pragma unroll
+      for (int e = 0; e < 8; ++e) pk.h[e] = __float2bfloat16((vals[8 * u + e] - m) * rstd);
+      const int cu = 4 * q + u;
+      zt8[p * 16 + (cu ^ (p & 7))] = pk.s;
+    }
+  }
+  __syncthreads();
+  const int lane = t & 63, wid = t >> 6;
+  const int wr = wid >> 1, wc = wid & 1;
+  const int ln = lane & 15, lq = lane >> 4;
+  f4v acc[2][2] = {};
+#pragma unroll
+  for (int kk = 0; kk < 4; ++kk) {
+    const int sl = (lq + 4 * kk) ^ (ln & 7);
+    s8v a[2], b[2];
+#pragma unroll
+    for (int mi = 0; mi < 2; ++mi) a[mi] = zt8[(32 * wr + 16 * mi + ln) * 16 + sl];
+#pragma unroll
+    for (int ni = 0; ni < 2; ++ni) b[ni] = w2s[(32 * wc + 16 * ni + ln) * 16 + sl];
+#pragma unroll
+    for (int mi = 0; mi < 2; ++mi)
+#pragma unroll
+      for (int ni = 0; ni < 2; ++ni) acc[mi][ni] = mfma16(a[mi], b[ni], acc[mi][ni]);
+  }
+#pragma unroll
+  for (int mi = 0; mi < 2; ++mi)
+#pragma unroll
+    for (int ni = 0; ni < 2; ++ni) {
+      const int col = 32 * wc + 16 * ni + ln;
+      const int jb = 32 * wr + 16 * mi + 4 * lq;
+      U4 o4;
+#pragma unroll
+      for (int r = 0; r < 4; ++r)
+        o4.h[r] = __float2bfloat16(acc[mi][ni][r] + bias2s[col] + betas[jb + r][col & 15]);
+      *(uint2*)&obuf[col][jb] = o4.u;
+    }
+  __syncthreads();
+  {
+    const int oc = t >> 2, js = (t & 3) * 16;
+    bf16* dp = bias_all + (size_t)oc * S * S + (size_t)i * S + j0 + js;
+    *(s8v*)dp = *(const s8v*)&obuf[oc][js];
+    *(s8v*)(dp + 8) = *(const s8v*)&obuf[oc][js + 8];
+  }
+}
+
+struct GemmAArgs {
+  const bf16* A0[2]; int lda0[2];
+  const bf16* A1[2]; int lda1[2];
+  const bf16* Bt[2];
+  const float* bias[2];
+  void* C[2];
+  int K[2]; int N[2]; int nb[2];
+  int amode[2]; int outMode[2];
+  bf16* vT;
+};
+
+DEV s8v combineRT(s8v x, s8v y, int amode) {
+  U8 ux, uy, rr;
+  ux.s = x; uy.s = y;
+#pragma unroll
+  for (int j = 0; j < 8; ++j) {
+    const float fx = __bfloat162float(ux.h[j]);
+    const float fy = __bfloat162float(uy.h[j]);
+    const float tt = sigmoidf_(fx);
+    rr.h[j] = __float2bfloat16((amode == 2 ? fx * tt : tt) * fy);
+  }
+  return rr.s;
+}
+
+__global__ __launch_bounds__(256) void gemmA(GemmAArgs ga) {
+  const int z = blockIdx.z;
+  if ((int)blockIdx.x >= ga.nb[z]) return;
+  __shared__ s8v As[512];
+  __shared__ s8v Bs[1024];
+  const bf16* A0 = ga.A0[z]; const int lda0 = ga.lda0[z];
+  const bf16* A1 = ga.A1[z]; const int lda1 = ga.lda1[z];
+  const bf16* Bt = ga.Bt[z];
+  const float* bias = ga.bias[z];
+  const int K = ga.K[z], N = ga.N[z], amode = ga.amode[z], om = ga.outMode[z];
+  const int t = threadIdx.x;
+  const int lane = t & 63, wid = t >> 6;
+  const int wr = wid >> 1, wc = wid & 1;
+  const int ln = lane & 15, lq = lane >> 4;
+  const int m0 = blockIdx.y * 64, n0 = blockIdx.x * 128;
+  int rowA[2], slA[2], swzA[2];
+#pragma unroll
+  for (int q = 0; q < 2; ++q) {
+    const int u = q * 256 + t;
+    rowA[q] = u >> 3; slA[q] = u & 7;
+    swzA[q] = rowA[q] * 8 + (slA[q] ^ (rowA[q] & 7));
+  }
+  int rowB[4], slB[4], swzB[4];
+#pragma unroll
+  for (int q = 0; q < 4; ++q) {
+    const int u = q * 256 + t;
+    rowB[q] = u >> 3; slB[q] = u & 7;
+    swzB[q] = rowB[q] * 8 + (slB[q] ^ (rowB[q] & 7));
+  }
+  f4v acc[2][4] = {};
+  s8v ra[2], ra2[2], rb[4];
+#pragma unroll
+  for (int q = 0; q < 2; ++q) {
+    ra[q] = *(const s8v*)(A0 + (size_t)(m0 + rowA[q]) * lda0 + slA[q] * 8);
+    if (amode != 0) ra2[q] = *(const s8v*)(A1 + (size_t)(m0 + rowA[q]) * lda1 + slA[q] * 8);
+  }
+#pragma unroll
+  for (int q = 0; q < 4; ++q)
+    rb[q] = *(const s8v*)(Bt + (size_t)(n0 + rowB[q]) * K + slB[q] * 8);
+  for (int ks = 0;;) {
+    __syncthreads();
+#pragma unroll
+    for (int q = 0; q < 2; ++q)
+      As[swzA[q]] = (amode == 0) ? ra[q] : combineRT(ra[q], ra2[q], amode);
+#pragma unroll
+    for (int q = 0; q < 4; ++q) Bs[swzB[q]] = rb[q];
+    const int ksn = ks + 64;
+    if (ksn < K) {
+#pragma unroll
+      for (int q = 0; q < 2; ++q) {
+        ra[q] = *(const s8v*)(A0 + (size_t)(m0 + rowA[q]) * lda0 + ksn + slA[q] * 8);
+        if (amode != 0) ra2[q] = *(const s8v*)(A1 + (size_t)(m0 + rowA[q]) * lda1 + ksn + slA[q] * 8);
+      }
+#pragma unroll
+      for (int q = 0; q < 4; ++q)
+        rb[q] = *(const s8v*)(Bt + (size_t)(n0 + rowB[q]) * K + ksn + slB[q] * 8);
+    }
+    __syncthreads();
+#pragma unroll
+    for (int kk = 0; kk < 2; ++kk) {
+      const int sl = (lq + 4 * kk) ^ (ln & 7);
+      s8v a[2], b[4];
+#pragma unroll
+      for (int mi = 0; mi < 2; ++mi) a[mi] = As[(32 * wr + 16 * mi + ln) * 8 + sl];
+#pragma unroll
+      for (int ni = 0; ni < 4; ++ni) b[ni] = Bs[(64 * wc + 16 * ni + ln) * 8 + sl];
+#pragma unroll
+      for (int mi = 0; mi < 2; ++mi)
+#pragma unroll
+        for (int ni = 0; ni < 4; ++ni) acc[mi][ni] = mfma16(a[mi], b[ni], acc[mi][ni]);
+    }
+    ks = ksn;
+    if (ks >= K) break;
+  }
+  const bool vdiv = (ga.vT != nullptr) && (z == 0) && (n0 >= 1536) && (n0 < 2304);
+#pragma unroll
+  for (int ni = 0; ni < 4; ++ni) {
+    const int n = n0 + 64 * wc + 16 * ni + ln;
+    const float bv = bias ? bias[n] : 0.f;
+#pragma unroll
+    for (int mi = 0; mi < 2; ++mi) {
+      const int mb = m0 + 32 * wr + 16 * mi + 4 * lq;
+      if (vdiv) {
+        U4 o4;
+#pragma unroll
+        for (int r = 0; r < 4; ++r) o4.h[r] = __float2bfloat16(acc[mi][ni][r] + bv);
+        *(uint2*)(ga.vT + (size_t)(n - 1536) * S + mb) = o4.u;
+      } else if (om == 0) {
+        bf16* Cb = (bf16*)ga.C[z];
+#pragma unroll
+        for (int r = 0; r < 4; ++r)
+          Cb[(size_t)(mb + r) * N + n] = __float2bfloat16(acc[mi][ni][r] + bv);
+      } else {
+        float* Cf = (float*)ga.C[z];
+#pragma unroll
+        for (int r = 0; r < 4; ++r)
+          Cf[(size_t)(mb + r) * N + n] = sigmoidf_(acc[mi][ni][r] + bv);
+      }
+    }
+  }
+}
+
+__global__ __launch_bounds__(256) void flash_split(const bf16* __restrict__ qkvg,
+                                                   const bf16* __restrict__ vT,
+                                                   const bf16* __restrict__ bias_all,
+                                                   float* __restrict__ opart,
+                                                   float* __restrict__ ml, int blk) {
+  __shared__ s8v Qs[64 * 8];
+  __shared__ s8v Ks[2][64 * 8];
+  __shared__ s8v Vs[2][48 * 8];
+  __shared__ s8v Bs[2][64 * 8];
+  __shared__ bf16 PwB[4 * 1024];
+  __shared__ float facL[4][16];
+  const int t = threadIdx.x;
+  const int lane = t & 63, w = t >> 6;
+  const int ln = lane & 15, lq = lane >> 4;
+  const int h = blockIdx.y, i0 = blockIdx.x * 64, half = blockIdx.z;
+  const bf16* bp = bias_all + (size_t)(blk * NHEAD + h) * S * S;
+  const float scale = 0.14433756729740643f;
+
+#pragma unroll
+  for (int uu = 0; uu < 2; ++uu) {
+    const int u = t + 256 * uu, row = u >> 3, sl = u & 7;
+    s8v qv{};
+    if (sl < 6) qv = *(const s8v*)(qkvg + (size_t)(i0 + row) * 3072 + h * DH + sl * 8);
+    Qs[row * 8 + (sl ^ (row & 7))] = qv;
+  }
+
+  s8v kr[2], br[2], vr0{}, vr1{};
+  auto prefetch = [&](int jt) {
+    const int j0 = jt * 64;
+#pragma unroll
+    for (int uu = 0; uu < 2; ++uu) {
+      const int u = t + 256 * uu, row = u >> 3, sl = u & 7;
+      s8v kv{};
+      if (sl < 6) kv = *(const s8v*)(qkvg + (size_t)(j0 + row) * 3072 + 768 + h * DH + sl * 8);
+      kr[uu] = kv;
+      br[uu] = *(const s8v*)(bp + (size_t)(i0 + row) * S + j0 + sl * 8);
+    }
+    { const int d = t >> 3, sl = t & 7;
+      vr0 = *(const s8v*)(vT + (size_t)(h * DH + d) * S + j0 + sl * 8); }
+    if (t < 128) {
+      const int u = 256 + t, d = u >> 3, sl = u & 7;
+      vr1 = *(const s8v*)(vT + (size_t)(h * DH + d) * S + j0 + sl * 8);
+    }
+  };
+  auto store_tiles = [&](int pb) {
+#pragma unroll
+    for (int uu = 0; uu < 2; ++uu) {
+      const int u = t + 256 * uu, row = u >> 3, sl = u & 7;
+      const int ph = row * 8 + (sl ^ (row & 7));
+      Ks[pb][ph] = kr[uu];
+      Bs[pb][ph] = br[uu];
+    }
+    { const int d = t >> 3, sl = t & 7;
+      Vs[pb][d * 8 + (sl ^ (d & 7))] = vr0; }
+    if (t < 128) {
+      const int u = 256 + t, d = u >> 3, sl = u & 7;
+      Vs[pb][d * 8 + (sl ^ (d & 7))] = vr1;
+    }
+  };
+
+  float m_run = -3e30f, l_run = 0.f;
+  f4v acc_o[3] = {};
+  bf16* pw = PwB + w * 1024;
+
+  prefetch(half * 8);
+  for (int jt2 = 0; jt2 < 8; ++jt2) {
+    const int pb = jt2 & 1;
+    __syncthreads();
+    store_tiles(pb);
+    __syncthreads();
+    if (jt2 < 7) prefetch(half * 8 + jt2 + 1);
+    float p[4][4];
+    float tmax = -3e30f;
+#pragma unroll
+    for (int ja = 0; ja < 4; ++ja) {
+      f4v accs = {};
+#pragma unroll
+      for (int ks2 = 0; ks2 < 2; ++ks2) {
+        const int sl = (lq + 4 * ks2) ^ (ln & 7);
+        const s8v a = Ks[pb][(16 * ja + ln) * 8 + sl];
+        const s8v b = Qs[(16 * w + ln) * 8 + sl];
+        accs = mfma16(a, b, accs);
+      }
+      const int jq = 4 * ja + lq;
+      const int pu = jq >> 1;
+      U4 bv;
+      bv.u = *(const uint2*)((const bf16*)(&Bs[pb][0]) +
+                             (((16 * w + ln) * 8 + (pu ^ (ln & 7))) * 8 + (jq & 1) * 4));
+#pragma unroll
+      for (int r = 0; r < 4; ++r) {
+        p[ja][r] = accs[r] * scale + __bfloat162float(bv.h[r]);
+        tmax = fmaxf(tmax, p[ja][r]);
+      }
+    }
+    tmax = fmaxf(tmax, __shfl_xor(tmax, 16));
+    tmax = fmaxf(tmax, __shfl_xor(tmax, 32));
+    const float m_new = fmaxf(m_run, tmax);
+    const float fac = __expf(m_run - m_new);
+    m_run = m_new;
+    float psum = 0.f;
+#pragma unroll
+    for (int ja = 0; ja < 4; ++ja)
+#pragma unroll
+      for (int r = 0; r < 4; ++r) {
+        p[ja][r] = __expf(p[ja][r] - m_new);
+        psum += p[ja][r];
+      }
+    psum += __shfl_xor(psum, 16);
+    psum += __shfl_xor(psum, 32);
+    l_run = l_run * fac + psum;
+    if (lq == 0) facL[w][ln] = fac;
+#pragma unroll
+    for (int ja = 0; ja < 4; ++ja) {
+      const int ju = 4 * ja + lq;
+      const int ph = ju ^ ((ln & 7) << 1);
+      U4 pk;
+#pragma unroll
+      for (int r = 0; r < 4; ++r) pk.h[r] = __float2bfloat16(p[ja][r]);
+      *(uint2*)(pw + ln * 64 + ph * 4) = pk.u;
+    }
+    asm volatile("s_waitcnt lgkmcnt(0)" ::: "memory");
+    __builtin_amdgcn_sched_barrier(0);
+    const float4 fv = *(const float4*)&facL[w][4 * lq];
+#pragma unroll
+    for (int ni = 0; ni < 3; ++ni) {
+      acc_o[ni][0] *= fv.x; acc_o[ni][1] *= fv.y;
+      acc_o[ni][2] *= fv.z; acc_o[ni][3] *= fv.w;
+    }
+#pragma unroll
+    for (int ks2 = 0; ks2 < 2; ++ks2) {
+      const int pu0 = (2 * lq + 8 * ks2) ^ ((ln & 7) << 1);
+      const s8v pa = *(const s8v*)(pw + ln * 64 + pu0 * 4);
+      const int slv = (lq + 4 * ks2) ^ (ln & 7);
+#pragma unroll
+      for (int ni = 0; ni < 3; ++ni) {
+        const s8v vb = Vs[pb][(16 * ni + ln) * 8 + slv];
+        acc_o[ni] = mfma16(pa, vb, acc_o[ni]);
+      }
+    }
+  }
+  if (lq == 0) {
+    ((float2*)ml)[(size_t)(half * NHEAD + h) * S + i0 + 16 * w + ln] =
+        make_float2(m_run, l_run);
+  }
+  float* op = opart + (size_t)half * S * CA;
+#pragma unroll
+  for (int ni = 0; ni < 3; ++ni)
+#pragma unroll
+    for (int r = 0; r < 4; ++r) {
+      const int m = i0 + 16 * w + 4 * lq + r;
+      op[(size_t)m * CA + h * DH + 16 * ni + ln] = acc_o[ni][r];
+    }
+}
+
+__global__ __launch_bounds__(256) void flash_combine(const float* __restrict__ opart,
+                                                     const float* __restrict__ ml,
+                                                     bf16* __restrict__ ob) {
+  const int row = blockIdx.x, t = threadIdx.x;
+  if (t >= 192) return;
+  const int c = 4 * t, h = t / 12;
+  const float2 a = ((const float2*)ml)[(size_t)h * S + row];
+  const float2 b = ((const float2*)ml)[(size_t)(NHEAD + h) * S + row];
+  const float M = fmaxf(a.x, b.x);
+  const float w1 = __expf(a.x - M), w2 = __expf(b.x - M);
+  const float inv = 1.0f / (w1 * a.y + w2 * b.y);
+  const float4 o1 = *(const float4*)(opart + (size_t)row * CA + c);
+  const float4 o2 = *(const float4*)(opart + (size_t)S * CA + (size_t)row * CA + c);
+  U4 o;
+  o.h[0] = __float2bfloat16((w1 * o1.x + w2 * o2.x) * inv);
+  o.h[1] = __float2bfloat16((w1 * o1.y + w2 * o2.y) * inv);
+  o.h[2] = __float2bfloat16((w1 * o1.z + w2 * o2.z) * inv);
+  o.h[3] = __float2bfloat16((w1 * o1.w + w2 * o2.w) * inv);
+  *(uint2*)(ob + (size_t)row * CA + c) = o.u;
 }
 
 __global__ void fill_kernel(float* p, int n, float v) {
@@ -723,6 +683,8 @@
   bf16* att = (bf16*)alloc((size_t)S * CA * 2);
   bf16* swg = (bf16*)alloc((size_t)S * 3072 * 2);
   bf16* trout = (bf16*)alloc((size_t)S * CA * 2);
+  float* opart = (float*)alloc((size_t)2 * S * CA * 4);
+  float* ml = (float*)alloc((size_t)2 * NHEAD * S * 8);
   if (used > ws_size) {
     fill_kernel<<<(out_size + 255) / 256, 256, 0, stream>>>((float*)d_out, out_size, 12345.0f);
     return;
@@ -768,38 +730,44 @@
   zbias_kernel<<<dim3(16, 1024), B256, 0, stream>>>(z_in, beta, W2T, bias2, bias_all);
 
   {
-    Gemm2Args ga{};
+    GemmAArgs ga{};
     ga.A0[0] = s_hat; ga.lda0[0] = 384; ga.Bt[0] = WT_ada; ga.bias[0] = nullptr;
-    ga.C[0] = ada_all; ga.K[0] = 384; ga.nb[0] = 96; ga.outMode[0] = 0; ga.N[0] = 12288;
+    ga.C[0] = ada_all; ga.K[0] = 384; ga.N[0] = 12288; ga.nb[0] = 96;
+    ga.amode[0] = 0; ga.outMode[0] = 0;
     ga.A0[1] = s_bf; ga.lda0[1] = 384; ga.Bt[1] = WT_sg; ga.bias[1] = biasSG;
-    ga.C[1] = sg_all; ga.K[1] = 384; ga.nb[1] = 48; ga.outMode[1] = 1; ga.N[1] = 6144;
+    ga.C[1] = sg_all; ga.K[1] = 384; ga.N[1] = 6144; ga.nb[1] = 48;
+    ga.amode[1] = 0; ga.outMode[1] = 1;
     ga.vT = nullptr;
-    gemm2<<<dim3(96, 8, 2), B256, 0, stream>>>(ga);
+    gemmA<<<dim3(96, 16, 2), B256, 0, stream>>>(ga);
   }
 
   ln_adaln2<<<S, B256, 0, stream>>>(a_in, ada_all, ah_attn, ah_tr);
   for (int b = 0; b < NBLK; ++b) {
     {
-      Gemm2Args ga{};
+      GemmAArgs ga{};
       ga.A0[0] = ah_attn; ga.lda0[0] = 768; ga.Bt[0] = WT_qkvg + (size_t)b * 3072 * 768;
-      ga.bias[0] = biasQKVG + b * 3072; ga.C[0] = qkvg; ga.K[0] = 768; ga.nb[0] = 24;
-      ga.outMode[0] = 0; ga.N[0] = 3072;
+      ga.bias[0] = biasQKVG + b * 3072; ga.C[0] = qkvg; ga.K[0] = 768; ga.N[0] = 3072;
+      ga.nb[0] = 24; ga.amode[0] = 0; ga.outMode[0] = 0;
       ga.A0[1] = ah_tr; ga.lda0[1] = 768; ga.Bt[1] = WT_mlp + (size_t)b * 3072 * 768;
-      ga.bias[1] = nullptr; ga.C[1] = swg; ga.K[1] = 768; ga.nb[1] = 24;
-      ga.outMode[1] = 0; ga.N[1] = 3072;
+      ga.bias[1] = nullptr; ga.C[1] = swg; ga.K[1] = 768; ga.N[1] = 3072;
+      ga.nb[1] = 24; ga.amode[1] = 0; ga.outMode[1] = 0;
       ga.vT = vT;
-      gemm2<<<dim3(24, 8, 2), B256, 0, stream>>>(ga);
-    }
-    flash_attn<<<dim3(16, 16), B256, 0, stream>>>(qkvg, vT, bias_all, ob, b);
+      gemmA<<<dim3(24, 16, 2), B256, 0, stream>>>(ga);
+    }
+    flash_split<<<dim3(16, 16, 2), B256, 0, stream>>>(qkvg, vT, bias_all, opart, ml, b);
+    flash_combine<<<S, B256, 0, stream>>>(opart, ml, ob);
     {
-      GemmPairArgs ga{};
+      GemmAArgs ga{};
       ga.A0[0] = qkvg + 2304; ga.lda0[0] = 3072; ga.A1[0] = ob; ga.lda1[0] = 768;
       ga.Bt[0] = WT_wo + (size_t)b * 768 * 768; ga.bias[0] = nullptr;
-      ga.C[0] = att; ga.K[0] = 768; ga.amode[0] = 1;
+      ga.C[0] = att; ga.K[0] = 768; ga.N[0] = 768; ga.nb[0] = 6;
+      ga.amode[0] = 1; ga.outMode[0] = 0;
       ga.A0[1] = swg; ga.lda0[1] = 3072; ga.A1[1] = swg + 1536; ga.lda1[1] = 3072;
       ga.Bt[1] = WT_wout + (size_t)b * 768 * 1536; ga.bias[1] = nullptr;
-      ga.C[1] = trout; ga.K[1] = 1536; ga.amode[1] = 2;
-      gemm_pair<<<dim3(6, 8, 2), B256, 0, stream>>>(ga, 768);
+      ga.C[1] = trout; ga.K[1] = 1536; ga.N[1] = 768; ga.nb[1] = 6;
+      ga.amode[1] = 2; ga.outMode[1] = 0;
+      ga.vT = nullptr;
+      gemmA<<<dim3(6, 16, 2), B256, 0, stream>>>(ga);
     }
     if (b < NBLK - 1) {
       final_adaln<<<S, B256, 0, stream>>>(sg_all + (size_t)b * 1536, att, trout,
```

Result: faster. 571.7 us (-15.5%).
